# Kernel optimization log

Measured on AMD Instinct MI355X. Metric: run time of the kernel, lower is better.

The kernel has to match this reference:

```python
import jax, jax.numpy as jnp
import numpy as np

D_MODEL = 256
D_STATE = 128          # d_model // 2
D_CONV = 4
EXPAND = 4
D_INNER = EXPAND * D_MODEL  # 1024
DT_RANK = (D_MODEL + 15) // 16  # 16
N_HEADS = 8
D_FF = 4 * D_MODEL
EPS = 1e-6


def layer_norm(x, a, b):
    # torch LayerNorm-like but with unbiased std (ddof=1) per the source
    mean = jnp.mean(x, axis=-1, keepdims=True)
    d = x.shape[-1]
    var = jnp.sum((x - mean) ** 2, axis=-1, keepdims=True) / (d - 1)
    std = jnp.sqrt(var)
    return a * (x - mean) / (std + EPS) + b


def silu(x):
    return x * jax.nn.sigmoid(x)


def mamba(x, in_proj_w, conv_w, conv_b, x_proj_w, dt_proj_w, dt_proj_b, A_log, Dp, out_proj_w):
    B, L, _ = x.shape
    xz = jnp.einsum('bld,ed->ble', x, in_proj_w)  # (B,L,2*D_INNER)
    xi, z = xz[..., :D_INNER], xz[..., D_INNER:]
    # causal depthwise conv1d over L
    xp = jnp.pad(xi, ((0, 0), (D_CONV - 1, 0), (0, 0)))
    u = conv_b
    for k in range(D_CONV):
        u = u + xp[:, k:k + L, :] * conv_w[:, k]
    u = silu(u)  # (B,L,D_INNER)
    dbl = jnp.einsum('bld,ed->ble', u, x_proj_w)  # (B,L,DT_RANK+2*D_STATE)
    dt = dbl[..., :DT_RANK]
    Bm = dbl[..., DT_RANK:DT_RANK + D_STATE]
    Cm = dbl[..., DT_RANK + D_STATE:]
    dt = jax.nn.softplus(jnp.einsum('blr,dr->bld', dt, dt_proj_w) + dt_proj_b)  # (B,L,D_INNER)
    A = -jnp.exp(A_log)  # (D_INNER, D_STATE)
    dA = jnp.exp(jnp.einsum('bld,dn->bldn', dt, A))          # (B,L,Din,N)
    dBu = jnp.einsum('bld,bln,bld->bldn', dt, Bm, u)          # (B,L,Din,N)

    def step(h, inp):
        dA_t, dBu_t, C_t = inp
        h = dA_t * h + dBu_t                    # (B,Din,N)
        y = jnp.einsum('bdn,bn->bd', h, C_t)    # (B,Din)
        return h, y

    h0 = jnp.zeros((B, D_INNER, D_STATE), dtype=x.dtype)
    _, ys = jax.lax.scan(step, h0, (jnp.swapaxes(dA, 0, 1), jnp.swapaxes(dBu, 0, 1), jnp.swapaxes(Cm, 0, 1)))
    y = jnp.swapaxes(ys, 0, 1) + u * Dp  # (B,L,Din)
    y = y * silu(z)
    return jnp.einsum('ble,de->bld', y, out_proj_w)


def cross_attention(q_in, kv_in, mask, wq_w, wq_b, wk_w, wk_b, wv_w, wv_b, wo_w, wo_b):
    B, Lq, _ = q_in.shape
    Lk = kv_in.shape[1]
    dk = D_MODEL // N_HEADS
    q = (jnp.einsum('bld,ed->ble', q_in, wq_w) + wq_b).reshape(B, Lq, N_HEADS, dk).transpose(0, 2, 1, 3)
    k = (jnp.einsum('bld,ed->ble', kv_in, wk_w) + wk_b).reshape(B, Lk, N_HEADS, dk).transpose(0, 2, 1, 3)
    v = (jnp.einsum('bld,ed->ble', kv_in, wv_w) + wv_b).reshape(B, Lk, N_HEADS, dk).transpose(0, 2, 1, 3)
    scores = jnp.einsum('bhqd,bhkd->bhqk', q, k) / np.sqrt(dk)
    # mask: (B,1,Lk) bool -> broadcast (B,1,1,Lk)
    scores = jnp.where(mask[:, None, :, :], scores, jnp.finfo(scores.dtype).min)
    p = jax.nn.softmax(scores, axis=-1)
    o = jnp.einsum('bhqk,bhkd->bhqd', p, v).transpose(0, 2, 1, 3).reshape(B, Lq, D_MODEL)
    return jnp.einsum('ble,de->bld', o, wo_w) + wo_b


def setup_inputs() -> dict:
    key = jax.random.key(0)
    ks = jax.random.split(key, 24)
    s = 0.02
    B, L, Lm = 2, 512, 512
    inp = {
        'x': jax.random.normal(ks[0], (B, L, D_MODEL), jnp.float32),
        'memory': jax.random.normal(ks[1], (B, Lm, D_MODEL), jnp.float32),
        'src_mask': jnp.ones((B, 1, Lm), bool),
        'tgt_mask': jnp.ones((B, 1, L), bool),
        # mamba params
        'in_proj_w': jax.random.normal(ks[2], (2 * D_INNER, D_MODEL)) * s,
        'conv_w': jax.random.normal(ks[3], (D_INNER, D_CONV)) * s,
        'conv_b': jnp.zeros((D_INNER,)),
        'x_proj_w': jax.random.normal(ks[4], (DT_RANK + 2 * D_STATE, D_INNER)) * s,
        'dt_proj_w': jax.random.normal(ks[5], (D_INNER, DT_RANK)) * s,
        'dt_proj_b': jnp.log(jnp.expm1(0.01)) * jnp.ones((D_INNER,)),
        'A_log': jnp.log(jnp.broadcast_to(jnp.arange(1, D_STATE + 1, dtype=jnp.float32), (D_INNER, D_STATE))),
        'Dp': jnp.ones((D_INNER,)),
        'out_proj_w': jax.random.normal(ks[6], (D_MODEL, D_INNER)) * s,
        # norms
        'norm1_a': jnp.ones((D_MODEL,)), 'norm1_b': jnp.zeros((D_MODEL,)),
        'norm2_a': jnp.ones((D_MODEL,)), 'norm2_b': jnp.zeros((D_MODEL,)),
        'norm3_a': jnp.ones((D_MODEL,)), 'norm3_b': jnp.zeros((D_MODEL,)),
        # cross attention
        'wq_w': jax.random.normal(ks[7], (D_MODEL, D_MODEL)) * s, 'wq_b': jnp.zeros((D_MODEL,)),
        'wk_w': jax.random.normal(ks[8], (D_MODEL, D_MODEL)) * s, 'wk_b': jnp.zeros((D_MODEL,)),
        'wv_w': jax.random.normal(ks[9], (D_MODEL, D_MODEL)) * s, 'wv_b': jnp.zeros((D_MODEL,)),
        'wo_w': jax.random.normal(ks[10], (D_MODEL, D_MODEL)) * s, 'wo_b': jnp.zeros((D_MODEL,)),
        # ffn
        'w1_w': jax.random.normal(ks[11], (D_FF, D_MODEL)) * s, 'w1_b': jnp.zeros((D_FF,)),
        'w2_w': jax.random.normal(ks[12], (D_MODEL, D_FF)) * s, 'w2_b': jnp.zeros((D_MODEL,)),
    }
    return inp


def reference(x, memory, src_mask, tgt_mask,
              in_proj_w, conv_w, conv_b, x_proj_w, dt_proj_w, dt_proj_b, A_log, Dp, out_proj_w,
              norm1_a, norm1_b, norm2_a, norm2_b, norm3_a, norm3_b,
              wq_w, wq_b, wk_w, wk_b, wv_w, wv_b, wo_w, wo_b,
              w1_w, w1_b, w2_w, w2_b):
    # self mamba block (pre-norm, residual); dropout = 0
    h = x + mamba(layer_norm(x, norm1_a, norm1_b), in_proj_w, conv_w, conv_b,
                  x_proj_w, dt_proj_w, dt_proj_b, A_log, Dp, out_proj_w)
    # cross attention block
    h = h + cross_attention(layer_norm(h, norm2_a, norm2_b), memory, src_mask,
                            wq_w, wq_b, wk_w, wk_b, wv_w, wv_b, wo_w, wo_b)
    # ffn block
    hn = layer_norm(h, norm3_a, norm3_b)
    ff = jnp.einsum('blf,df->bld', jax.nn.relu(jnp.einsum('bld,fd->blf', hn, w1_w) + w1_b), w2_w) + w2_b
    return h + ff
```

## Files before the change

kernel.cpp:

```cpp
#include <hip/hip_runtime.h>
#include <hip/hip_bf16.h>

#define B_SZ 2
#define L_SEQ 512
#define D_MODEL 256
#define D_STATE 128
#define D_CONV 4
#define D_INNER 1024
#define DT_RANK 16
#define N_HEADS 8
#define DK 32
#define D_FF 1024
#define R_TOT (B_SZ * L_SEQ)
#define DBL_LD (DT_RANK + 2 * D_STATE)
#define NSEG 16
#define SEGL 32
#define DPB 4

typedef __hip_bfloat16 bf16;
typedef __attribute__((ext_vector_type(8))) short short8;
typedef __attribute__((ext_vector_type(4))) float floatx4;

__device__ inline float fexp(float x) { return __expf(x); }
__device__ inline float fexp2(float x) { return __builtin_amdgcn_exp2f(x); }
__device__ inline float frcp(float x) { return __builtin_amdgcn_rcpf(x); }
__device__ inline float silu_f(float x) { return x * frcp(1.f + fexp(-x)); }
__device__ inline float softplus_f(float x) { return (x > 20.f) ? x : __logf(1.f + fexp(x)); }
__device__ inline float bf2f(unsigned short u) { return __uint_as_float(((unsigned)u) << 16); }

__device__ inline float dpp_sum64(float x) {
    x += __int_as_float(__builtin_amdgcn_update_dpp(0, __float_as_int(x), 0x111, 0xf, 0xf, true));
    x += __int_as_float(__builtin_amdgcn_update_dpp(0, __float_as_int(x), 0x112, 0xf, 0xf, true));
    x += __int_as_float(__builtin_amdgcn_update_dpp(0, __float_as_int(x), 0x114, 0xf, 0xf, true));
    x += __int_as_float(__builtin_amdgcn_update_dpp(0, __float_as_int(x), 0x118, 0xf, 0xf, true));
    x += __int_as_float(__builtin_amdgcn_update_dpp(0, __float_as_int(x), 0x142, 0xf, 0xf, true));
    x += __int_as_float(__builtin_amdgcn_update_dpp(0, __float_as_int(x), 0x143, 0xf, 0xf, true));
    return x;
}

__device__ inline float swz_xor16(float x) {
    return __int_as_float(__builtin_amdgcn_ds_swizzle(__float_as_int(x), 0x401F));
}
__device__ inline float swz_xor8(float x) {
    return __int_as_float(__builtin_amdgcn_ds_swizzle(__float_as_int(x), 0x201F));
}

#define S_MEM 262144
#define S_INW 524288
#define S_XPW 278528
#define S_OPW 262144
#define S_WQ  65536
#define S_WK  65536
#define S_WV  65536
#define S_WO  65536
#define S_W1  262144
#define S_W2  262144
#define S_TOT (S_MEM+S_INW+S_XPW+S_OPW+S_WQ+S_WK+S_WV+S_WO+S_W1+S_W2)
#define PACK_BLKS ((S_TOT + 255) / 256)
#define Z1_F4 (4 * R_TOT * D_MODEL / 4)
#define Z2_F4 (R_TOT * D_MODEL / 4)
#define Z3_F4 (R_TOT * DBL_LD / 4)
#define ZERO_BLKS ((Z1_F4 + Z2_F4 + Z3_F4 + 255) / 256)

__global__ __launch_bounds__(256) void pack_ln1(
    const float* __restrict__ s0, const float* __restrict__ s1,
    const float* __restrict__ s2, const float* __restrict__ s3,
    const float* __restrict__ s4, const float* __restrict__ s5,
    const float* __restrict__ s6, const float* __restrict__ s7,
    const float* __restrict__ s8, const float* __restrict__ s9,
    bf16* __restrict__ dst,
    const float* __restrict__ X, const float* __restrict__ a,
    const float* __restrict__ bvec, bf16* __restrict__ ln1b,
    float* __restrict__ zero1, float* __restrict__ zero2,
    float* __restrict__ zero3)
{
    __shared__ float r1[256], r2[256];
    if (blockIdx.x < PACK_BLKS) {
        const long i = (long)blockIdx.x * 256 + threadIdx.x;
        if (i >= S_TOT) return;
        const long off[11] = {0, S_MEM, S_MEM+S_INW, S_MEM+S_INW+S_XPW,
            S_MEM+S_INW+S_XPW+S_OPW, S_MEM+S_INW+S_XPW+S_OPW+S_WQ,
            S_MEM+S_INW+S_XPW+S_OPW+S_WQ+S_WK,
            S_MEM+S_INW+S_XPW+S_OPW+S_WQ+S_WK+S_WV,
            S_MEM+S_INW+S_XPW+S_OPW+S_WQ+S_WK+S_WV+S_WO,
            S_MEM+S_INW+S_XPW+S_OPW+S_WQ+S_WK+S_WV+S_WO+S_W1, S_TOT};
        const float* srcs[10] = {s0,s1,s2,s3,s4,s5,s6,s7,s8,s9};
        int seg = 0;
#pragma unroll
        for (int k = 1; k < 10; ++k) if (i >= off[k]) seg = k;
        dst[i] = __float2bfloat16(srcs[seg][i - off[seg]]);
    } else if (blockIdx.x < PACK_BLKS + R_TOT) {
        const int row = blockIdx.x - PACK_BLKS;
        const int t = threadIdx.x;
        const float v = X[(long)row * D_MODEL + t];
        r1[t] = v;
        r2[t] = v * v;
        __syncthreads();
        for (int s = 128; s > 0; s >>= 1) {
            if (t < s) { r1[t] += r1[t + s]; r2[t] += r2[t + s]; }
            __syncthreads();
        }
        const float mean = r1[0] * (1.f / 256.f);
        const float var = (r2[0] - 256.f * mean * mean) * (1.f / 255.f);
        const float sd = sqrtf(fmaxf(var, 0.f));
        const float o = a[t] * (v - mean) / (sd + 1e-6f) + bvec[t];
        ln1b[(long)row * D_MODEL + t] = __float2bfloat16(o);
    } else {
        const long i4 = (long)(blockIdx.x - PACK_BLKS - R_TOT) * 256 + threadIdx.x;
        const float4 z = {0.f, 0.f, 0.f, 0.f};
        if (i4 < Z1_F4)                      *(float4*)&zero1[i4 * 4] = z;
        else if (i4 < Z1_F4 + Z2_F4)          *(float4*)&zero2[(i4 - Z1_F4) * 4] = z;
        else if (i4 < Z1_F4 + Z2_F4 + Z3_F4)  *(float4*)&zero3[(i4 - Z1_F4 - Z2_F4) * 4] = z;
    }
}

template <int EPI>
__global__ __launch_bounds__(256) void mfma_gemm(
    const bf16* __restrict__ A, const bf16* __restrict__ W, int K,
    float* __restrict__ C, bf16* __restrict__ Cb, int ldc,
    const float* __restrict__ bias, const float* __restrict__ res,
    int M, int N)
{
    const int wave = threadIdx.x >> 6;
    const int lane = threadIdx.x & 63;
    const int row16 = lane & 15;
    const int quad  = lane >> 4;
    const int bm = blockIdx.y * 64 + wave * 16;
    const int bn = blockIdx.x * 64;

    floatx4 acc[4];
#pragma unroll
    for (int t = 0; t < 4; ++t) acc[t] = (floatx4){0.f, 0.f, 0.f, 0.f};

    const long arow = (long)(bm + row16) * K;
    for (int k0 = 0; k0 < K; k0 += 32) {
        const short8 av = *(const short8*)(A + arow + k0 + quad * 8);
#pragma unroll
        for (int t = 0; t < 4; ++t) {
            const int gn = bn + t * 16 + row16;
            short8 bv = {0,0,0,0,0,0,0,0};
            if (gn < N) bv = *(const short8*)(W + (long)gn * K + k0 + quad * 8);
            acc[t] = __builtin_amdgcn_mfma_f32_16x16x32_bf16(av, bv, acc[t], 0, 0, 0);
        }
    }

#pragma unroll
    for (int t = 0; t < 4; ++t) {
        const int gn = bn + t * 16 + row16;
        if (gn >= N) continue;
        const float bs = bias ? bias[gn] : 0.f;
#pragma unroll
        for (int r = 0; r < 4; ++r) {
            const int gm = bm + quad * 4 + r;
            float v = acc[t][r] + bs;
            if (EPI == 1) v = fmaxf(v, 0.f);
            const long ci = (long)gm * ldc + gn;
            if (res) v += res[ci];
            if (C)  C[ci] = v;
            if (Cb) Cb[ci] = __float2bfloat16(v);
        }
    }
}

template <int SK>
__global__ __launch_bounds__(256) void splitk_gemm(
    const bf16* __restrict__ A, const bf16* __restrict__ W, int K,
    float* __restrict__ C, int ldc,
    const float* __restrict__ bias, const float* __restrict__ res,
    int M, int N)
{
    const int wave = threadIdx.x >> 6;
    const int lane = threadIdx.x & 63;
    const int row16 = lane & 15;
    const int quad  = lane >> 4;
    const int bm = blockIdx.y * 64 + wave * 16;
    const int bn = blockIdx.x * 64;
    const int kz = blockIdx.z;
    const int ksl = K / SK;
    const int kbeg = kz * ksl;

    floatx4 acc[4];
#pragma unroll
    for (int t = 0; t < 4; ++t) acc[t] = (floatx4){0.f, 0.f, 0.f, 0.f};

    const long arow = (long)(bm + row16) * K;
    for (int k0 = kbeg; k0 < kbeg + ksl; k0 += 32) {
        const short8 av = *(const short8*)(A + arow + k0 + quad * 8);
#pragma unroll
        for (int t = 0; t < 4; ++t) {
            const int gn = bn + t * 16 + row16;
            short8 bv = {0,0,0,0,0,0,0,0};
            if (gn < N) bv = *(const short8*)(W + (long)gn * K + k0 + quad * 8);
            acc[t] = __builtin_amdgcn_mfma_f32_16x16x32_bf16(av, bv, acc[t], 0, 0, 0);
        }
    }

#pragma unroll
    for (int t = 0; t < 4; ++t) {
        const int gn = bn + t * 16 + row16;
        if (gn >= N) continue;
        const float bs = (kz == 0 && bias) ? bias[gn] : 0.f;
#pragma unroll
        for (int r = 0; r < 4; ++r) {
            const int gm = bm + quad * 4 + r;
            float v = acc[t][r] + bs;
            const long ci = (long)gm * ldc + gn;
            if (kz == 0 && res) v += res[ci];
            atomicAdd(&C[ci], v);
        }
    }
}

__global__ __launch_bounds__(256) void xproj_kv_gemm(
    const bf16* __restrict__ ub, const bf16* __restrict__ XPWb,
    float* __restrict__ dbl,
    const bf16* __restrict__ memb, const bf16* __restrict__ WKb,
    const bf16* __restrict__ WVb,
    const float* __restrict__ WKB, const float* __restrict__ WVB,
    float* __restrict__ kb, float* __restrict__ vb)
{
    const int wave = threadIdx.x >> 6;
    const int lane = threadIdx.x & 63;
    const int row16 = lane & 15;
    const int quad  = lane >> 4;
    const int bm = blockIdx.y * 64 + wave * 16;
    const int bn = blockIdx.x * 64;
    const int z = blockIdx.z;

    const bf16* A; const bf16* W; const float* bias; float* C;
    int K, N, ldc, kbeg, ksl;
    if (z < 4) {
        A = ub; W = XPWb; bias = nullptr; C = dbl;
        K = D_INNER; N = DBL_LD; ldc = DBL_LD;
        ksl = D_INNER / 4; kbeg = z * ksl;
    } else {
        if (bn >= D_MODEL) return;
        const int zz = z - 4;
        const int which = zz >> 1;
        const int kz = zz & 1;
        A = memb; W = which ? WVb : WKb;
        bias = (kz == 0) ? (which ? WVB : WKB) : nullptr;
        C = which ? vb : kb;
        K = D_MODEL; N = D_MODEL; ldc = D_MODEL;
        ksl = D_MODEL / 2; kbeg = kz * ksl;
    }

    floatx4 acc[4];
#pragma unroll
    for (int t = 0; t < 4; ++t) acc[t] = (floatx4){0.f, 0.f, 0.f, 0.f};

    const long arow = (long)(bm + row16) * K;
    for (int k0 = kbeg; k0 < kbeg + ksl; k0 += 32) {
        const short8 av = *(const short8*)(A + arow + k0 + quad * 8);
#pragma unroll
        for (int t = 0; t < 4; ++t) {
            const int gn = bn + t * 16 + row16;
            short8 bv = {0,0,0,0,0,0,0,0};
            if (gn < N) bv = *(const short8*)(W + (long)gn * K + k0 + quad * 8);
            acc[t] = __builtin_amdgcn_mfma_f32_16x16x32_bf16(av, bv, acc[t], 0, 0, 0);
        }
    }

#pragma unroll
    for (int t = 0; t < 4; ++t) {
        const int gn = bn + t * 16 + row16;
        if (gn >= N) continue;
        const float bs = bias ? bias[gn] : 0.f;
#pragma unroll
        for (int r = 0; r < 4; ++r) {
            const int gm = bm + quad * 4 + r;
            atomicAdd(&C[(long)gm * ldc + gn], acc[t][r] + bs);
        }
    }
}

__global__ __launch_bounds__(256) void q_gemm(
    const bf16* __restrict__ ln2b, const bf16* __restrict__ WQb,
    const float* __restrict__ WQB, float* __restrict__ qb)
{
    const int wave = threadIdx.x >> 6;
    const int lane = threadIdx.x & 63;
    const int row16 = lane & 15;
    const int quad  = lane >> 4;
    const int bm = blockIdx.y * 64 + wave * 16;
    const int bn = blockIdx.x * 64;
    const int kz = blockIdx.z;
    const int kbeg = kz * (D_MODEL / 2);

    floatx4 acc[4];
#pragma unroll
    for (int t = 0; t < 4; ++t) acc[t] = (floatx4){0.f, 0.f, 0.f, 0.f};

    const long arow = (long)(bm + row16) * D_MODEL;
    for (int k0 = kbeg; k0 < kbeg + D_MODEL / 2; k0 += 32) {
        const short8 av = *(const short8*)(ln2b + arow + k0 + quad * 8);
#pragma unroll
        for (int t = 0; t < 4; ++t) {
            const int gn = bn + t * 16 + row16;
            const short8 bv = *(const short8*)(WQb + (long)gn * D_MODEL + k0 + quad * 8);
            acc[t] = __builtin_amdgcn_mfma_f32_16x16x32_bf16(av, bv, acc[t], 0, 0, 0);
        }
    }
#pragma unroll
    for (int t = 0; t < 4; ++t) {
        const int gn = bn + t * 16 + row16;
        const float bs = (kz == 0) ? WQB[gn] : 0.f;
#pragma unroll
        for (int r = 0; r < 4; ++r) {
            const int gm = bm + quad * 4 + r;
            atomicAdd(&qb[(long)gm * D_MODEL + gn], acc[t][r] + bs);
        }
    }
}

__global__ __launch_bounds__(256) void gemm16_ln(
    const bf16* __restrict__ A, const bf16* __restrict__ W, int K,
    const float* __restrict__ bias, const float* __restrict__ res,
    float* __restrict__ Cf,
    const float* __restrict__ lna, const float* __restrict__ lnb,
    bf16* __restrict__ lnout)
{
    __shared__ float tile[16][264];
    __shared__ float red1[16][16];
    __shared__ float red2[16][16];
    const int w = threadIdx.x >> 6;
    const int lane = threadIdx.x & 63;
    const int row16 = lane & 15;
    const int quad  = lane >> 4;
    const int bm = blockIdx.x * 16;

    floatx4 acc[4];
#pragma unroll
    for (int t = 0; t < 4; ++t) acc[t] = (floatx4){0.f, 0.f, 0.f, 0.f};

    const long arow = (long)(bm + row16) * K;
    for (int k0 = 0; k0 < K; k0 += 32) {
        const short8 av = *(const short8*)(A + arow + k0 + quad * 8);
#pragma unroll
        for (int t = 0; t < 4; ++t) {
            const int gn = w * 64 + t * 16 + row16;
            const short8 bv = *(const short8*)(W + (long)gn * K + k0 + quad * 8);
            acc[t] = __builtin_amdgcn_mfma_f32_16x16x32_bf16(av, bv, acc[t], 0, 0, 0);
        }
    }

#pragma unroll
    for (int t = 0; t < 4; ++t) {
        const int gn = w * 64 + t * 16 + row16;
        const float bs = bias ? bias[gn] : 0.f;
#pragma unroll
        for (int r = 0; r < 4; ++r) {
            const int gm = bm + quad * 4 + r;
            float v = acc[t][r] + bs;
            const long ci = (long)gm * D_MODEL + gn;
            if (res) v += res[ci];
            Cf[ci] = v;
            tile[quad * 4 + r][gn] = v;
        }
    }
    __syncthreads();

    const int r = threadIdx.x >> 4;
    const int g = threadIdx.x & 15;
    float s = 0.f, q = 0.f;
#pragma unroll
    for (int i = 0; i < 16; ++i) {
        const float x = tile[r][g * 16 + i];
        s += x; q += x * x;
    }
    red1[r][g] = s; red2[r][g] = q;
    __syncthreads();
    float ts = 0.f, tq = 0.f;
#pragma unroll
    for (int i = 0; i < 16; ++i) { ts += red1[r][i]; tq += red2[r][i]; }
    const float mean = ts * (1.f / 256.f);
    const float var = (tq - 256.f * mean * mean) * (1.f / 255.f);
    const float sd = sqrtf(fmaxf(var, 0.f));
    const long rowbase = (long)(bm + r) * D_MODEL;
#pragma unroll
    for (int i = 0; i < 16; ++i) {
        const int c = g * 16 + i;
        const float o = lna[c] * (tile[r][c] - mean) / (sd + 1e-6f) + lnb[c];
        lnout[rowbase + c] = __float2bfloat16(o);
    }
}

__global__ __launch_bounds__(256) void ln_kernel(
    const float* __restrict__ x, const float* __restrict__ a,
    const float* __restrict__ bvec, bf16* __restrict__ out)
{
    const int row = blockIdx.x;
    const int t = threadIdx.x;
    const float v = x[(long)row * D_MODEL + t];
    __shared__ float r1[256], r2[256];
    r1[t] = v;
    r2[t] = v * v;
    __syncthreads();
    for (int s = 128; s > 0; s >>= 1) {
        if (t < s) { r1[t] += r1[t + s]; r2[t] += r2[t + s]; }
        __syncthreads();
    }
    const float mean = r1[0] * (1.f / 256.f);
    const float var = (r2[0] - 256.f * mean * mean) * (1.f / 255.f);
    const float sd = sqrtf(fmaxf(var, 0.f));
    const float o = a[t] * (v - mean) / (sd + 1e-6f) + bvec[t];
    out[(long)row * D_MODEL + t] = __float2bfloat16(o);
}

__global__ __launch_bounds__(256) void dt_gemm_T(
    const float* __restrict__ A , const float* __restrict__ W ,
    const float* __restrict__ bias, float* __restrict__ dtT)
{
    __shared__ float As[DT_RANK][65];
    __shared__ float Bs[DT_RANK][65];
    __shared__ float Ct[64][65];
    const int bm = blockIdx.y * 64;
    const int bn = blockIdx.x * 64;
    const int tid = threadIdx.x;
    const int tx = tid & 15;
    const int ty = tid >> 4;
    const int r = tid >> 2;
    const int kk = (tid & 3) * 4;
#pragma unroll
    for (int q = 0; q < 4; ++q) {
        As[kk + q][r] = A[(long)(bm + r) * DBL_LD + kk + q];
        Bs[kk + q][r] = W[(long)(bn + r) * DT_RANK + kk + q];
    }
    __syncthreads();
    float acc[4][4] = {};
#pragma unroll
    for (int k = 0; k < DT_RANK; ++k) {
        float a[4], bv[4];
#pragma unroll
        for (int i = 0; i < 4; ++i) a[i] = As[k][ty * 4 + i];
#pragma unroll
        for (int j = 0; j < 4; ++j) bv[j] = Bs[k][tx * 4 + j];
#pragma unroll
        for (int i = 0; i < 4; ++i)
#pragma unroll
            for (int j = 0; j < 4; ++j)
                acc[i][j] = fmaf(a[i], bv[j], acc[i][j]);
    }
#pragma unroll
    for (int i = 0; i < 4; ++i)
#pragma unroll
        for (int j = 0; j < 4; ++j)
            Ct[tx * 4 + j][ty * 4 + i] = softplus_f(acc[i][j] + bias[bn + tx * 4 + j]);
    __syncthreads();
    const int b = bm >> 9;
    const int l0 = bm & 511;
    const int r2 = tid >> 4;
    const int c4 = (tid & 15) * 4;
#pragma unroll
    for (int q = 0; q < 4; ++q) {
        const int dl = r2 + q * 16;
        float4 v = {Ct[dl][c4], Ct[dl][c4 + 1], Ct[dl][c4 + 2], Ct[dl][c4 + 3]};
        *(float4*)&dtT[((long)(b * D_INNER + bn + dl) << 9) + l0 + c4] = v;
    }
}

__global__ __launch_bounds__(256) void conv_silu_T(
    const bf16* __restrict__ xz, const float* __restrict__ cw,
    const float* __restrict__ cb, bf16* __restrict__ ub, float* __restrict__ uT)
{
    __shared__ float t[64][65];
    const int db = blockIdx.x;
    const int lb = blockIdx.y;
    const int b  = blockIdx.z;
    const int tid = threadIdx.x;
    const int r  = tid >> 4;
    const int c4 = (tid & 15) * 4;
    const int d0 = db * 64 + c4;

    const float4 cb4 = *(const float4*)&cb[d0];
    float cwa[4][4];
#pragma unroll
    for (int i = 0; i < 4; ++i) {
        const float4 w = *(const float4*)&cw[(d0 + i) * 4];
        cwa[i][0] = w.x; cwa[i][1] = w.y; cwa[i][2] = w.z; cwa[i][3] = w.w;
    }

#pragma unroll
    for (int q = 0; q < 4; ++q) {
        const int ll = r + q * 16;
        const int l = lb * 64 + ll;
        float s0 = cb4.x, s1 = cb4.y, s2 = cb4.z, s3 = cb4.w;
#pragma unroll
        for (int k = 0; k < D_CONV; ++k) {
            const int ls = l - 3 + k;
            if (ls >= 0) {
                const ushort4 xv = *(const ushort4*)&xz[((long)(b * L_SEQ + ls)) * (2 * D_INNER) + d0];
                s0 = fmaf(bf2f(xv.x), cwa[0][k], s0);
                s1 = fmaf(bf2f(xv.y), cwa[1][k], s1);
                s2 = fmaf(bf2f(xv.z), cwa[2][k], s2);
                s3 = fmaf(bf2f(xv.w), cwa[3][k], s3);
            }
        }
        s0 = silu_f(s0); s1 = silu_f(s1); s2 = silu_f(s2); s3 = silu_f(s3);
        bf16 b0 = __float2bfloat16(s0), b1 = __float2bfloat16(s1);
        bf16 b2 = __float2bfloat16(s2), b3 = __float2bfloat16(s3);
        ushort4 pk;
        pk.x = *reinterpret_cast<unsigned short*>(&b0);
        pk.y = *reinterpret_cast<unsigned short*>(&b1);
        pk.z = *reinterpret_cast<unsigned short*>(&b2);
        pk.w = *reinterpret_cast<unsigned short*>(&b3);
        *reinterpret_cast<ushort4*>(ub + ((long)(b * L_SEQ + l)) * D_INNER + d0) = pk;
        t[c4 + 0][ll] = s0; t[c4 + 1][ll] = s1;
        t[c4 + 2][ll] = s2; t[c4 + 3][ll] = s3;
    }
    __syncthreads();
#pragma unroll
    for (int q = 0; q < 4; ++q) {
        const int dl = r + q * 16;
        float4 v = {t[dl][c4], t[dl][c4 + 1], t[dl][c4 + 2], t[dl][c4 + 3]};
        *(float4*)&uT[((long)(b * D_INNER + db * 64 + dl) << 9) + lb * 64 + c4] = v;
    }
}

__global__ __launch_bounds__(1024) void scan_fused(
    const float* __restrict__ dtT, const float* __restrict__ uT,
    const float* __restrict__ dbl, const float* __restrict__ A_log,
    float* __restrict__ ysT)
{
    const int b  = blockIdx.x >> 8;
    const int d0 = (blockIdx.x & 255) * DPB;
    const int w = threadIdx.x >> 6;
    const int lane = threadIdx.x & 63;
    const int n0 = lane * 2;

    __shared__ float Sh[NSEG][DPB][D_STATE];
    __shared__ float Ph[NSEG][DPB][D_STATE];

    float An0[DPB], An1[DPB];
#pragma unroll
    for (int di = 0; di < DPB; ++di) {
        An0[di] = -fexp(A_log[(long)(d0 + di) * D_STATE + n0]) * 1.44269504f;
        An1[di] = -fexp(A_log[(long)(d0 + di) * D_STATE + n0 + 1]) * 1.44269504f;
    }

    const float* blp = dbl + ((long)(b * L_SEQ + w * SEGL)) * DBL_LD + DT_RANK + n0;
    const float* clp = blp + D_STATE;
    const long tbase = ((long)(b * D_INNER + d0) << 9) + w * SEGL;

    if (w < NSEG - 1) {
        float h0[DPB] = {}, h1[DPB] = {}, sdt[DPB] = {};
        for (int s = 0; s < SEGL / 8; ++s) {
            float2 Bv[8];
#pragma unroll
            for (int j = 0; j < 8; ++j)
                Bv[j] = *(const float2*)(blp + (long)(s * 8 + j) * DBL_LD);
#pragma unroll
            for (int di = 0; di < DPB; ++di) {
                const float* dtp = dtT + tbase + ((long)di << 9) + s * 8;
                const float* up  = uT  + tbase + ((long)di << 9) + s * 8;
                const float4 dt0 = *(const float4*)dtp;
                const float4 dt1 = *(const float4*)(dtp + 4);
                const float4 u0  = *(const float4*)up;
                const float4 u1  = *(const float4*)(up + 4);
                const float dts[8] = {dt0.x, dt0.y, dt0.z, dt0.w, dt1.x, dt1.y, dt1.z, dt1.w};
                const float us[8]  = {u0.x,  u0.y,  u0.z,  u0.w,  u1.x,  u1.y,  u1.z,  u1.w};
#pragma unroll
                for (int j = 0; j < 8; ++j) {
                    const float dtv = dts[j];
                    sdt[di] += dtv;
                    const float dtu = dtv * us[j];
                    h0[di] = fmaf(fexp2(dtv * An0[di]), h0[di], dtu * Bv[j].x);
                    h1[di] = fmaf(fexp2(dtv * An1[di]), h1[di], dtu * Bv[j].y);
                }
            }
        }
#pragma unroll
        for (int di = 0; di < DPB; ++di) {
            Sh[w][di][n0]     = h0[di];
            Sh[w][di][n0 + 1] = h1[di];
            Ph[w][di][n0]     = fexp2(An0[di] * sdt[di]);
            Ph[w][di][n0 + 1] = fexp2(An1[di] * sdt[di]);
        }
    }
    __syncthreads();

    float h0[DPB] = {}, h1[DPB] = {};
    for (int s = 0; s < w; ++s) {
#pragma unroll
        for (int di = 0; di < DPB; ++di) {
            h0[di] = fmaf(Ph[s][di][n0],     h0[di], Sh[s][di][n0]);
            h1[di] = fmaf(Ph[s][di][n0 + 1], h1[di], Sh[s][di][n0 + 1]);
        }
    }

    const int bpa = (lane ^ 32) << 2;
    const bool lo32 = lane < 32;
    const bool b16 = (lane & 16) != 0;
    const bool b8  = (lane & 8) != 0;
    const int g = lane >> 3;
    const bool wl = (lane & 7) == 7;

    for (int s = 0; s < SEGL / 8; ++s) {
        float2 Bv[8], Cv[8];
#pragma unroll
        for (int j = 0; j < 8; ++j) {
            Bv[j] = *(const float2*)(blp + (long)(s * 8 + j) * DBL_LD);
            Cv[j] = *(const float2*)(clp + (long)(s * 8 + j) * DBL_LD);
        }
#pragma unroll
        for (int di = 0; di < DPB; ++di) {
            const float* dtp = dtT + tbase + ((long)di << 9) + s * 8;
            const float* up  = uT  + tbase + ((long)di << 9) + s * 8;
            const float4 dt0 = *(const float4*)dtp;
            const float4 dt1 = *(const float4*)(dtp + 4);
            const float4 u0  = *(const float4*)up;
            const float4 u1  = *(const float4*)(up + 4);
            const float dts[8] = {dt0.x, dt0.y, dt0.z, dt0.w, dt1.x, dt1.y, dt1.z, dt1.w};
            const float us[8]  = {u0.x,  u0.y,  u0.z,  u0.w,  u1.x,  u1.y,  u1.z,  u1.w};
            float yp[8];
#pragma unroll
            for (int j = 0; j < 8; ++j) {
                const float dtv = dts[j];
                const float dtu = dtv * us[j];
                h0[di] = fmaf(fexp2(dtv * An0[di]), h0[di], dtu * Bv[j].x);
                h1[di] = fmaf(fexp2(dtv * An1[di]), h1[di], dtu * Bv[j].y);
                yp[j] = fmaf(h0[di], Cv[j].x, h1[di] * Cv[j].y);
            }
            float z0[4];
#pragma unroll
            for (int j = 0; j < 4; ++j) {
                const float t = lo32 ? yp[j]     : yp[j + 4];
                const float u = lo32 ? yp[j + 4] : yp[j];
                z0[j] = t + __int_as_float(
                    __builtin_amdgcn_ds_bpermute(bpa, __float_as_int(u)));
            }
            float z1[2];
#pragma unroll
            for (int j = 0; j < 2; ++j) {
                const float t = b16 ? z0[j + 2] : z0[j];
                const float u = b16 ? z0[j]     : z0[j + 2];
                z1[j] = t + swz_xor16(u);
            }
            float z2;
            {
                const float t = b8 ? z1[1] : z1[0];
                const float u = b8 ? z1[0] : z1[1];
                z2 = t + swz_xor8(u);
            }
            z2 += __int_as_float(__builtin_amdgcn_update_dpp(0, __float_as_int(z2), 0x111, 0xf, 0xf, true));
            z2 += __int_as_float(__builtin_amdgcn_update_dpp(0, __float_as_int(z2), 0x112, 0xf, 0xf, true));
            z2 += __int_as_float(__builtin_amdgcn_update_dpp(0, __float_as_int(z2), 0x114, 0xf, 0xf, true));
            if (wl) ysT[tbase + ((long)di << 9) + s * 8 + g] = z2;
        }
    }
}

__global__ __launch_bounds__(256) void gate_kernel(
    const float* __restrict__ ysT, const float* __restrict__ uT,
    const float* __restrict__ Dp, const bf16* __restrict__ xz,
    bf16* __restrict__ y)
{
    __shared__ float t[64][65];
    __shared__ float t2[64][65];
    const int db = blockIdx.x;
    const int lb = blockIdx.y;
    const int b  = blockIdx.z;
    const int tid = threadIdx.x;
    const int r  = tid >> 4;
    const int c4 = (tid & 15) * 4;

#pragma unroll
    for (int q = 0; q < 4; ++q) {
        const int dr = r + q * 16;
        const long base = (((long)(b * D_INNER + db * 64 + dr)) << 9) + lb * 64 + c4;
        const float4 v = *(const float4*)&ysT[base];
        const float4 w = *(const float4*)&uT[base];
        t[dr][c4 + 0] = v.x; t[dr][c4 + 1] = v.y;
        t[dr][c4 + 2] = v.z; t[dr][c4 + 3] = v.w;
        t2[dr][c4 + 0] = w.x; t2[dr][c4 + 1] = w.y;
        t2[dr][c4 + 2] = w.z; t2[dr][c4 + 3] = w.w;
    }
    __syncthreads();

    const float4 dp4 = *(const float4*)&Dp[db * 64 + c4];
#pragma unroll
    for (int q = 0; q < 4; ++q) {
        const int lr = r + q * 16;
        const long row = (long)b * L_SEQ + lb * 64 + lr;
        const ushort4 zu = *(const ushort4*)&xz[row * 2 * D_INNER + D_INNER + db * 64 + c4];
        const float r0 = (t[c4 + 0][lr] + t2[c4 + 0][lr] * dp4.x) * silu_f(bf2f(zu.x));
        const float r1 = (t[c4 + 1][lr] + t2[c4 + 1][lr] * dp4.y) * silu_f(bf2f(zu.y));
        const float r2 = (t[c4 + 2][lr] + t2[c4 + 2][lr] * dp4.z) * silu_f(bf2f(zu.z));
        const float r3 = (t[c4 + 3][lr] + t2[c4 + 3][lr] * dp4.w) * silu_f(bf2f(zu.w));
        bf16 b0 = __float2bfloat16(r0), b1 = __float2bfloat16(r1);
        bf16 b2 = __float2bfloat16(r2), b3 = __float2bfloat16(r3);
        ushort4 pk;
        pk.x = *reinterpret_cast<unsigned short*>(&b0);
        pk.y = *reinterpret_cast<unsigned short*>(&b1);
        pk.z = *reinterpret_cast<unsigned short*>(&b2);
        pk.w = *reinterpret_cast<unsigned short*>(&b3);
        *reinterpret_cast<ushort4*>(y + row * D_INNER + db * 64 + c4) = pk;
    }
}

#define QT 16
#define CK 64

__global__ __launch_bounds__(256) void attn_kernel(
    const float* __restrict__ q, const float* __restrict__ k,
    const float* __restrict__ v, bf16* __restrict__ o)
{
    const int qt = blockIdx.x;
    const int hh = blockIdx.y;
    const int b  = blockIdx.z;
    const int t = threadIdx.x;
    const int lane = t & 15;
    const int qa = t >> 4;
    const int q0 = qt * QT + qa;

    __shared__ float Ks[CK][36];
    __shared__ float Vs[CK][36];

    const float scale = 0.17677669529663687f;
    float qr0[32];
    {
        const float* q0p = q + ((long)(b * L_SEQ + q0) * D_MODEL + hh * DK);
#pragma unroll
        for (int i = 0; i < 8; ++i) {
            const float4 a = *(const float4*)&q0p[i * 4];
            qr0[i*4+0] = a.x * scale; qr0[i*4+1] = a.y * scale;
            qr0[i*4+2] = a.z * scale; qr0[i*4+3] = a.w * scale;
        }
    }

    float m0 = -1e30f, l0 = 0.f, o0[32] = {};

    for (int c = 0; c < L_SEQ; c += CK) {
        __syncthreads();
        {
            const int fid = t * 2;
            const int row = fid >> 3;
            const int c0  = (fid & 7) * 4;
            const float* kp = k + ((long)(b * L_SEQ + c + row) * D_MODEL + hh * DK + c0);
            const float* vp = v + ((long)(b * L_SEQ + c + row) * D_MODEL + hh * DK + c0);
            *(float4*)&Ks[row][c0]     = *(const float4*)kp;
            *(float4*)&Ks[row][c0 + 4] = *(const float4*)(kp + 4);
            *(float4*)&Vs[row][c0]     = *(const float4*)vp;
            *(float4*)&Vs[row][c0 + 4] = *(const float4*)(vp + 4);
        }
        __syncthreads();

        float s0[4];
#pragma unroll
        for (int i = 0; i < 4; ++i) {
            const int kk = i * 16 + lane;
            float a0 = 0.f;
#pragma unroll
            for (int dd = 0; dd < 32; dd += 4) {
                const float4 kv = *(const float4*)&Ks[kk][dd];
                a0 = fmaf(qr0[dd+0], kv.x, a0); a0 = fmaf(qr0[dd+1], kv.y, a0);
                a0 = fmaf(qr0[dd+2], kv.z, a0); a0 = fmaf(qr0[dd+3], kv.w, a0);
            }
            s0[i] = a0;
        }

        float cm0 = s0[0];
#pragma unroll
        for (int i = 1; i < 4; ++i) cm0 = fmaxf(cm0, s0[i]);
#pragma unroll
        for (int off = 8; off > 0; off >>= 1)
            cm0 = fmaxf(cm0, __shfl_down(cm0, off, 16));
        cm0 = __shfl(cm0, 0, 16);

        const float nm0 = fmaxf(m0, cm0);
        const float al0 = fexp(m0 - nm0);
        l0 *= al0;
#pragma unroll
        for (int dd = 0; dd < 32; ++dd) o0[dd] *= al0;
        m0 = nm0;

        float p0[4];
#pragma unroll
        for (int i = 0; i < 4; ++i) { p0[i] = fexp(s0[i] - m0); l0 += p0[i]; }

#pragma unroll
        for (int i = 0; i < 4; ++i) {
            const int kk = i * 16 + lane;
#pragma unroll
            for (int dd = 0; dd < 32; dd += 4) {
                const float4 vv = *(const float4*)&Vs[kk][dd];
                o0[dd+0] = fmaf(p0[i], vv.x, o0[dd+0]);
                o0[dd+1] = fmaf(p0[i], vv.y, o0[dd+1]);
                o0[dd+2] = fmaf(p0[i], vv.z, o0[dd+2]);
                o0[dd+3] = fmaf(p0[i], vv.w, o0[dd+3]);
            }
        }
    }

#pragma unroll
    for (int off = 8; off > 0; off >>= 1) {
        l0 += __shfl_down(l0, off, 16);
#pragma unroll
        for (int dd = 0; dd < 32; ++dd) o0[dd] += __shfl_down(o0[dd], off, 16);
    }
    if (lane == 0) {
        const float i0 = 1.f / l0;
        bf16* op0 = o + ((long)(b * L_SEQ + q0) * D_MODEL + hh * DK);
#pragma unroll
        for (int dd = 0; dd < 32; ++dd) op0[dd] = __float2bfloat16(o0[dd] * i0);
    }
}


extern "C" void kernel_launch(void* const* d_in, const int* in_sizes, int n_in,
                              void* d_out, int out_size, void* d_ws, size_t ws_size,
                              hipStream_t stream) {
    const float* X   = (const float*)d_in[0];
    const float* MEM = (const float*)d_in[1];
    const float* CW  = (const float*)d_in[5];
    const float* CB  = (const float*)d_in[6];
    const float* DTW = (const float*)d_in[8];
    const float* DTB = (const float*)d_in[9];
    const float* ALG = (const float*)d_in[10];
    const float* DP  = (const float*)d_in[11];
    const float* N1A = (const float*)d_in[13];
    const float* N1B = (const float*)d_in[14];
    const float* N2A = (const float*)d_in[15];
    const float* N2B = (const float*)d_in[16];
    const float* N3A = (const float*)d_in[17];
    const float* N3B = (const float*)d_in[18];
    const float* WQB = (const float*)d_in[20];
    const float* WKB = (const float*)d_in[22];
    const float* WVB = (const float*)d_in[24];
    const float* WOB = (const float*)d_in[26];
    const float* W1B = (const float*)d_in[28];
    const float* W2B = (const float*)d_in[30];
    const float* INW = (const float*)d_in[4];
    const float* XPW = (const float*)d_in[7];
    const float* OPW = (const float*)d_in[12];
    const float* WQ  = (const float*)d_in[19];
    const float* WKw = (const float*)d_in[21];
    const float* WVw = (const float*)d_in[23];
    const float* WO  = (const float*)d_in[25];
    const float* W1  = (const float*)d_in[27];
    const float* W2  = (const float*)d_in[29];
    float* out = (float*)d_out;

    bf16* bp = (bf16*)d_ws;
    bf16* ub   = bp;  bp += (long)R_TOT * D_INNER;
    bf16* ybb  = bp;  bp += (long)R_TOT * D_INNER;
    bf16* ffab = ybb;
    bf16* xzb  = bp;  bp += (long)R_TOT * 2 * D_INNER;
    bf16* ln1b = bp;  bp += (long)R_TOT * D_MODEL;
    bf16* aob  = ln1b;
    bf16* ln2b = bp;  bp += (long)R_TOT * D_MODEL;
    bf16* ln3b = ln2b;
    bf16* arena = bp; bp += S_TOT;
    bf16* MEMb = arena;
    bf16* INWb = MEMb + S_MEM;
    bf16* XPWb = INWb + S_INW;
    bf16* OPWb = XPWb + S_XPW;
    bf16* WQb  = OPWb + S_OPW;
    bf16* WKb  = WQb + S_WQ;
    bf16* WVb  = WKb + S_WK;
    bf16* WOb  = WVb + S_WV;
    bf16* W1b  = WOb + S_WO;
    bf16* W2b  = W1b + S_W1;

    float* p = (float*)(bp + ((((long)(bp - (bf16*)d_ws)) & 1) ? 1 : 0));
    float* uT  = p;                                  p += (long)R_TOT * D_INNER;
    float* dbl = p;                                  p += (long)R_TOT * DBL_LD;
    float* dtT = p;                                  p += (long)R_TOT * D_INNER;
    float* ysT = p;                                  p += (long)R_TOT * D_INNER;
    float* h1  = p;                                  p += (long)R_TOT * D_MODEL;
    float* qb  = p;                                  p += (long)R_TOT * D_MODEL;
    float* kb  = p;                                  p += (long)R_TOT * D_MODEL;
    float* vb  = p;                                  p += (long)R_TOT * D_MODEL;
    float* h2  = p;                                  p += (long)R_TOT * D_MODEL;

    const dim3 blk256(256);
    const int MT64 = R_TOT / 64;

    pack_ln1<<<PACK_BLKS + R_TOT + ZERO_BLKS, blk256, 0, stream>>>(
        MEM, INW, XPW, OPW, WQ, WKw, WVw, WO, W1, W2, arena,
        X, N1A, N1B, ln1b, h1, out, dbl);

    mfma_gemm<0><<<dim3(2 * D_INNER / 64, MT64), blk256, 0, stream>>>(
        ln1b, INWb, D_MODEL, nullptr, xzb, 2 * D_INNER, nullptr, nullptr,
        R_TOT, 2 * D_INNER);

    conv_silu_T<<<dim3(D_INNER / 64, L_SEQ / 64, B_SZ), blk256, 0, stream>>>(
        xzb, CW, CB, ub, uT);

    xproj_kv_gemm<<<dim3((DBL_LD + 63) / 64, MT64, 8), blk256, 0, stream>>>(
        ub, XPWb, dbl, MEMb, WKb, WVb, WKB, WVB, kb, vb);

    dt_gemm_T<<<dim3(D_INNER / 64, MT64), blk256, 0, stream>>>(dbl, DTW, DTB, dtT);

    scan_fused<<<B_SZ * D_INNER / DPB, dim3(1024), 0, stream>>>(dtT, uT, dbl, ALG, ysT);

    gate_kernel<<<dim3(D_INNER / 64, L_SEQ / 64, B_SZ), blk256, 0, stream>>>(
        ysT, uT, DP, xzb, ybb);

    splitk_gemm<4><<<dim3(D_MODEL / 64, MT64, 4), blk256, 0, stream>>>(
        ybb, OPWb, D_INNER, h1, D_MODEL, nullptr, X, R_TOT, D_MODEL);

    ln_kernel<<<R_TOT, blk256, 0, stream>>>(h1, N2A, N2B, ln2b);

    q_gemm<<<dim3(D_MODEL / 64, MT64, 2), blk256, 0, stream>>>(ln2b, WQb, WQB, qb);

    attn_kernel<<<dim3(L_SEQ / QT, N_HEADS, B_SZ), blk256, 0, stream>>>(qb, kb, vb, aob);

    gemm16_ln<<<R_TOT / 16, blk256, 0, stream>>>(
        aob, WOb, D_MODEL, WOB, h1, h2, N3A, N3B, ln3b);

    mfma_gemm<1><<<dim3(D_FF / 64, MT64), blk256, 0, stream>>>(
        ln3b, W1b, D_MODEL, nullptr, ffab, D_FF, W1B, nullptr, R_TOT, D_FF);

    splitk_gemm<4><<<dim3(D_MODEL / 64, MT64, 4), blk256, 0, stream>>>(
        ffab, W2b, D_FF, out, D_MODEL, W2B, h2, R_TOT, D_MODEL);

    (void)in_sizes; (void)n_in; (void)out_size; (void)ws_size;
}
```

Baseline: 321.8 us.

## Merge pre-scan and post-scan kernel chains into two cooperative persistent kernels

Replaces the chain of separate launches before the scan (pack/LN1, in_proj GEMM, conv+SiLU, x_proj/KV GEMM, dt GEMM) and after it (gate, out_proj, LN2, Q, attention, WO+LN3, FFN) with two cooperative kernels. Inside each, grid-stride loops run the former stages and grid.sync() separates them. The goal is to cut kernel launch overhead and inter-kernel gaps across the many small stages. In exchange, the grid is capped by occupancy, each stage runs at one fixed grid size and shared-memory footprint, and grid-wide barriers add their own cost.

```diff
diff --git a/kernel.cpp b/kernel.cpp
--- a/kernel.cpp
+++ b/kernel.cpp
@@ -1,5 +1,8 @@
 #include <hip/hip_runtime.h>
 #include <hip/hip_bf16.h>
+#include <hip/hip_cooperative_groups.h>
+
+namespace cg = cooperative_groups;
 
 #define B_SZ 2
 #define L_SEQ 512
@@ -28,21 +31,29 @@
 __device__ inline float softplus_f(float x) { return (x > 20.f) ? x : __logf(1.f + fexp(x)); }
 __device__ inline float bf2f(unsigned short u) { return __uint_as_float(((unsigned)u) << 16); }
 
-__device__ inline float dpp_sum64(float x) {
-    x += __int_as_float(__builtin_amdgcn_update_dpp(0, __float_as_int(x), 0x111, 0xf, 0xf, true));
-    x += __int_as_float(__builtin_amdgcn_update_dpp(0, __float_as_int(x), 0x112, 0xf, 0xf, true));
-    x += __int_as_float(__builtin_amdgcn_update_dpp(0, __float_as_int(x), 0x114, 0xf, 0xf, true));
-    x += __int_as_float(__builtin_amdgcn_update_dpp(0, __float_as_int(x), 0x118, 0xf, 0xf, true));
-    x += __int_as_float(__builtin_amdgcn_update_dpp(0, __float_as_int(x), 0x142, 0xf, 0xf, true));
-    x += __int_as_float(__builtin_amdgcn_update_dpp(0, __float_as_int(x), 0x143, 0xf, 0xf, true));
-    return x;
-}
-
 __device__ inline float swz_xor16(float x) {
     return __int_as_float(__builtin_amdgcn_ds_swizzle(__float_as_int(x), 0x401F));
 }
 __device__ inline float swz_xor8(float x) {
     return __int_as_float(__builtin_amdgcn_ds_swizzle(__float_as_int(x), 0x201F));
+}
+
+__device__ inline void gemm64_body(const bf16* A, const bf16* W, int K,
+    int kbeg, int kend, int bm, int bn, int N, floatx4 acc[4], int lane)
+{
+    const int row16 = lane & 15;
+    const int quad  = lane >> 4;
+    const long arow = (long)(bm + row16) * K;
+    for (int k0 = kbeg; k0 < kend; k0 += 32) {
+        const short8 av = *(const short8*)(A + arow + k0 + quad * 8);
+#pragma unroll
+        for (int t = 0; t < 4; ++t) {
+            const int gn = bn + t * 16 + row16;
+            short8 bv = {0,0,0,0,0,0,0,0};
+            if (gn < N) bv = *(const short8*)(W + (long)gn * K + k0 + quad * 8);
+            acc[t] = __builtin_amdgcn_mfma_f32_16x16x32_bf16(av, bv, acc[t], 0, 0, 0);
+        }
+    }
 }
 
 #define S_MEM 262144
@@ -62,458 +73,237 @@
 #define Z3_F4 (R_TOT * DBL_LD / 4)
 #define ZERO_BLKS ((Z1_F4 + Z2_F4 + Z3_F4 + 255) / 256)
 
-__global__ __launch_bounds__(256) void pack_ln1(
-    const float* __restrict__ s0, const float* __restrict__ s1,
-    const float* __restrict__ s2, const float* __restrict__ s3,
-    const float* __restrict__ s4, const float* __restrict__ s5,
-    const float* __restrict__ s6, const float* __restrict__ s7,
-    const float* __restrict__ s8, const float* __restrict__ s9,
-    bf16* __restrict__ dst,
-    const float* __restrict__ X, const float* __restrict__ a,
-    const float* __restrict__ bvec, bf16* __restrict__ ln1b,
-    float* __restrict__ zero1, float* __restrict__ zero2,
-    float* __restrict__ zero3)
+__global__ __launch_bounds__(256, 4) void head_fused(
+    const float* s0, const float* s1, const float* s2, const float* s3,
+    const float* s4, const float* s5, const float* s6, const float* s7,
+    const float* s8, const float* s9,
+    bf16* arena,
+    const float* X, const float* n1a, const float* n1b, bf16* ln1b,
+    float* z1, float* z2, float* z3,
+    const bf16* INWb, bf16* xzb,
+    const float* CW, const float* CB, bf16* ub, float* uT,
+    const bf16* XPWb, float* dbl,
+    const bf16* MEMb, const bf16* WKb, const bf16* WVb,
+    const float* WKB, const float* WVB, float* kb, float* vbuf,
+    const float* DTW, const float* DTB, float* dtT)
 {
-    __shared__ float r1[256], r2[256];
-    if (blockIdx.x < PACK_BLKS) {
-        const long i = (long)blockIdx.x * 256 + threadIdx.x;
-        if (i >= S_TOT) return;
-        const long off[11] = {0, S_MEM, S_MEM+S_INW, S_MEM+S_INW+S_XPW,
-            S_MEM+S_INW+S_XPW+S_OPW, S_MEM+S_INW+S_XPW+S_OPW+S_WQ,
-            S_MEM+S_INW+S_XPW+S_OPW+S_WQ+S_WK,
-            S_MEM+S_INW+S_XPW+S_OPW+S_WQ+S_WK+S_WV,
-            S_MEM+S_INW+S_XPW+S_OPW+S_WQ+S_WK+S_WV+S_WO,
-            S_MEM+S_INW+S_XPW+S_OPW+S_WQ+S_WK+S_WV+S_WO+S_W1, S_TOT};
-        const float* srcs[10] = {s0,s1,s2,s3,s4,s5,s6,s7,s8,s9};
-        int seg = 0;
-#pragma unroll
-        for (int k = 1; k < 10; ++k) if (i >= off[k]) seg = k;
-        dst[i] = __float2bfloat16(srcs[seg][i - off[seg]]);
-    } else if (blockIdx.x < PACK_BLKS + R_TOT) {
-        const int row = blockIdx.x - PACK_BLKS;
-        const int t = threadIdx.x;
-        const float v = X[(long)row * D_MODEL + t];
-        r1[t] = v;
-        r2[t] = v * v;
-        __syncthreads();
-        for (int s = 128; s > 0; s >>= 1) {
-            if (t < s) { r1[t] += r1[t + s]; r2[t] += r2[t + s]; }
-            __syncthreads();
-        }
-        const float mean = r1[0] * (1.f / 256.f);
-        const float var = (r2[0] - 256.f * mean * mean) * (1.f / 255.f);
-        const float sd = sqrtf(fmaxf(var, 0.f));
-        const float o = a[t] * (v - mean) / (sd + 1e-6f) + bvec[t];
-        ln1b[(long)row * D_MODEL + t] = __float2bfloat16(o);
-    } else {
-        const long i4 = (long)(blockIdx.x - PACK_BLKS - R_TOT) * 256 + threadIdx.x;
-        const float4 z = {0.f, 0.f, 0.f, 0.f};
-        if (i4 < Z1_F4)                      *(float4*)&zero1[i4 * 4] = z;
-        else if (i4 < Z1_F4 + Z2_F4)          *(float4*)&zero2[(i4 - Z1_F4) * 4] = z;
-        else if (i4 < Z1_F4 + Z2_F4 + Z3_F4)  *(float4*)&zero3[(i4 - Z1_F4 - Z2_F4) * 4] = z;
-    }
-}
-
-template <int EPI>
-__global__ __launch_bounds__(256) void mfma_gemm(
-    const bf16* __restrict__ A, const bf16* __restrict__ W, int K,
-    float* __restrict__ C, bf16* __restrict__ Cb, int ldc,
-    const float* __restrict__ bias, const float* __restrict__ res,
-    int M, int N)
-{
-    const int wave = threadIdx.x >> 6;
-    const int lane = threadIdx.x & 63;
+    cg::grid_group gg = cg::this_grid();
+    __shared__ float sm[6240];
+    const int tid = threadIdx.x;
+    const int NB = (int)gridDim.x;
+    const int lane = tid & 63;
+    const int wave = tid >> 6;
     const int row16 = lane & 15;
     const int quad  = lane >> 4;
-    const int bm = blockIdx.y * 64 + wave * 16;
-    const int bn = blockIdx.x * 64;
-
-    floatx4 acc[4];
-#pragma unroll
-    for (int t = 0; t < 4; ++t) acc[t] = (floatx4){0.f, 0.f, 0.f, 0.f};
-
-    const long arow = (long)(bm + row16) * K;
-    for (int k0 = 0; k0 < K; k0 += 32) {
-        const short8 av = *(const short8*)(A + arow + k0 + quad * 8);
+
+    {
+        const int TOTB = PACK_BLKS + R_TOT + ZERO_BLKS;
+        for (int vb0 = (int)blockIdx.x; vb0 < TOTB; vb0 += NB) {
+            if (vb0 < PACK_BLKS) {
+                const long i = (long)vb0 * 256 + tid;
+                if (i < S_TOT) {
+                    const long off[11] = {0, S_MEM, S_MEM+S_INW, S_MEM+S_INW+S_XPW,
+                        S_MEM+S_INW+S_XPW+S_OPW, S_MEM+S_INW+S_XPW+S_OPW+S_WQ,
+                        S_MEM+S_INW+S_XPW+S_OPW+S_WQ+S_WK,
+                        S_MEM+S_INW+S_XPW+S_OPW+S_WQ+S_WK+S_WV,
+                        S_MEM+S_INW+S_XPW+S_OPW+S_WQ+S_WK+S_WV+S_WO,
+                        S_MEM+S_INW+S_XPW+S_OPW+S_WQ+S_WK+S_WV+S_WO+S_W1, S_TOT};
+                    const float* srcs[10] = {s0,s1,s2,s3,s4,s5,s6,s7,s8,s9};
+                    int seg = 0;
+#pragma unroll
+                    for (int k = 1; k < 10; ++k) if (i >= off[k]) seg = k;
+                    arena[i] = __float2bfloat16(srcs[seg][i - off[seg]]);
+                }
+            } else if (vb0 < PACK_BLKS + R_TOT) {
+                float* r1 = sm; float* r2 = sm + 256;
+                const int row = vb0 - PACK_BLKS;
+                const float v = X[(long)row * D_MODEL + tid];
+                r1[tid] = v; r2[tid] = v * v;
+                __syncthreads();
+                for (int s = 128; s > 0; s >>= 1) {
+                    if (tid < s) { r1[tid] += r1[tid + s]; r2[tid] += r2[tid + s]; }
+                    __syncthreads();
+                }
+                const float mean = r1[0] * (1.f / 256.f);
+                const float var = (r2[0] - 256.f * mean * mean) * (1.f / 255.f);
+                const float sd = sqrtf(fmaxf(var, 0.f));
+                const float o = n1a[tid] * (v - mean) / (sd + 1e-6f) + n1b[tid];
+                ln1b[(long)row * D_MODEL + tid] = __float2bfloat16(o);
+                __syncthreads();
+            } else {
+                const long i4 = (long)(vb0 - PACK_BLKS - R_TOT) * 256 + tid;
+                const float4 zz = {0.f, 0.f, 0.f, 0.f};
+                if (i4 < Z1_F4)                      *(float4*)&z1[i4 * 4] = zz;
+                else if (i4 < Z1_F4 + Z2_F4)          *(float4*)&z2[(i4 - Z1_F4) * 4] = zz;
+                else if (i4 < Z1_F4 + Z2_F4 + Z3_F4)  *(float4*)&z3[(i4 - Z1_F4 - Z2_F4) * 4] = zz;
+            }
+        }
+    }
+    gg.sync();
+
+    for (int vb0 = (int)blockIdx.x; vb0 < 512; vb0 += NB) {
+        const int bn = (vb0 & 31) * 64;
+        const int bm = (vb0 >> 5) * 64 + wave * 16;
+        floatx4 acc[4];
+#pragma unroll
+        for (int t = 0; t < 4; ++t) acc[t] = (floatx4){0.f, 0.f, 0.f, 0.f};
+        gemm64_body(ln1b, INWb, D_MODEL, 0, D_MODEL, bm, bn, 2 * D_INNER, acc, lane);
 #pragma unroll
         for (int t = 0; t < 4; ++t) {
             const int gn = bn + t * 16 + row16;
-            short8 bv = {0,0,0,0,0,0,0,0};
-            if (gn < N) bv = *(const short8*)(W + (long)gn * K + k0 + quad * 8);
-            acc[t] = __builtin_amdgcn_mfma_f32_16x16x32_bf16(av, bv, acc[t], 0, 0, 0);
-        }
-    }
-
-#pragma unroll
-    for (int t = 0; t < 4; ++t) {
-        const int gn = bn + t * 16 + row16;
-        if (gn >= N) continue;
-        const float bs = bias ? bias[gn] : 0.f;
-#pragma unroll
-        for (int r = 0; r < 4; ++r) {
-            const int gm = bm + quad * 4 + r;
-            float v = acc[t][r] + bs;
-            if (EPI == 1) v = fmaxf(v, 0.f);
-            const long ci = (long)gm * ldc + gn;
-            if (res) v += res[ci];
-            if (C)  C[ci] = v;
-            if (Cb) Cb[ci] = __float2bfloat16(v);
-        }
-    }
-}
-
-template <int SK>
-__global__ __launch_bounds__(256) void splitk_gemm(
-    const bf16* __restrict__ A, const bf16* __restrict__ W, int K,
-    float* __restrict__ C, int ldc,
-    const float* __restrict__ bias, const float* __restrict__ res,
-    int M, int N)
-{
-    const int wave = threadIdx.x >> 6;
-    const int lane = threadIdx.x & 63;
-    const int row16 = lane & 15;
-    const int quad  = lane >> 4;
-    const int bm = blockIdx.y * 64 + wave * 16;
-    const int bn = blockIdx.x * 64;
-    const int kz = blockIdx.z;
-    const int ksl = K / SK;
-    const int kbeg = kz * ksl;
-
-    floatx4 acc[4];
-#pragma unroll
-    for (int t = 0; t < 4; ++t) acc[t] = (floatx4){0.f, 0.f, 0.f, 0.f};
-
-    const long arow = (long)(bm + row16) * K;
-    for (int k0 = kbeg; k0 < kbeg + ksl; k0 += 32) {
-        const short8 av = *(const short8*)(A + arow + k0 + quad * 8);
+#pragma unroll
+            for (int r = 0; r < 4; ++r) {
+                const int gm = bm + quad * 4 + r;
+                xzb[(long)gm * (2 * D_INNER) + gn] = __float2bfloat16(acc[t][r]);
+            }
+        }
+    }
+    gg.sync();
+
+    for (int vb0 = (int)blockIdx.x; vb0 < 256; vb0 += NB) {
+        float (*tt)[65] = (float(*)[65])sm;
+        const int db = vb0 & 15;
+        const int lb = (vb0 >> 4) & 7;
+        const int b  = vb0 >> 7;
+        const int r  = tid >> 4;
+        const int c4 = (tid & 15) * 4;
+        const int d0 = db * 64 + c4;
+
+        const float4 cb4 = *(const float4*)&CB[d0];
+        float cwa[4][4];
+#pragma unroll
+        for (int i = 0; i < 4; ++i) {
+            const float4 w4 = *(const float4*)&CW[(d0 + i) * 4];
+            cwa[i][0] = w4.x; cwa[i][1] = w4.y; cwa[i][2] = w4.z; cwa[i][3] = w4.w;
+        }
+#pragma unroll
+        for (int q = 0; q < 4; ++q) {
+            const int ll = r + q * 16;
+            const int l = lb * 64 + ll;
+            float v0 = cb4.x, v1 = cb4.y, v2 = cb4.z, v3 = cb4.w;
+#pragma unroll
+            for (int k = 0; k < D_CONV; ++k) {
+                const int ls = l - 3 + k;
+                if (ls >= 0) {
+                    const ushort4 xv = *(const ushort4*)&xzb[((long)(b * L_SEQ + ls)) * (2 * D_INNER) + d0];
+                    v0 = fmaf(bf2f(xv.x), cwa[0][k], v0);
+                    v1 = fmaf(bf2f(xv.y), cwa[1][k], v1);
+                    v2 = fmaf(bf2f(xv.z), cwa[2][k], v2);
+                    v3 = fmaf(bf2f(xv.w), cwa[3][k], v3);
+                }
+            }
+            v0 = silu_f(v0); v1 = silu_f(v1); v2 = silu_f(v2); v3 = silu_f(v3);
+            bf16 b0 = __float2bfloat16(v0), b1 = __float2bfloat16(v1);
+            bf16 b2 = __float2bfloat16(v2), b3 = __float2bfloat16(v3);
+            ushort4 pk;
+            pk.x = *reinterpret_cast<unsigned short*>(&b0);
+            pk.y = *reinterpret_cast<unsigned short*>(&b1);
+            pk.z = *reinterpret_cast<unsigned short*>(&b2);
+            pk.w = *reinterpret_cast<unsigned short*>(&b3);
+            *reinterpret_cast<ushort4*>(ub + ((long)(b * L_SEQ + l)) * D_INNER + d0) = pk;
+            tt[c4 + 0][ll] = v0; tt[c4 + 1][ll] = v1;
+            tt[c4 + 2][ll] = v2; tt[c4 + 3][ll] = v3;
+        }
+        __syncthreads();
+#pragma unroll
+        for (int q = 0; q < 4; ++q) {
+            const int dl = r + q * 16;
+            float4 v = {tt[dl][c4], tt[dl][c4 + 1], tt[dl][c4 + 2], tt[dl][c4 + 3]};
+            *(float4*)&uT[((long)(b * D_INNER + db * 64 + dl) << 9) + lb * 64 + c4] = v;
+        }
+        __syncthreads();
+    }
+    gg.sync();
+
+    for (int vb0 = (int)blockIdx.x; vb0 < 640; vb0 += NB) {
+        const int xib = vb0 % 5;
+        const int yib = (vb0 / 5) & 15;
+        const int z   = vb0 / 80;
+        const int bm = yib * 64 + wave * 16;
+        const int bn = xib * 64;
+
+        const bf16* A; const bf16* W; const float* bias; float* C;
+        int K, N, ldc, kbeg, ksl;
+        if (z < 4) {
+            A = ub; W = XPWb; bias = nullptr; C = dbl;
+            K = D_INNER; N = DBL_LD; ldc = DBL_LD;
+            ksl = D_INNER / 4; kbeg = z * ksl;
+        } else {
+            if (bn >= D_MODEL) continue;
+            const int zz = z - 4;
+            const int which = zz >> 1;
+            const int kz = zz & 1;
+            A = MEMb; W = which ? WVb : WKb;
+            bias = (kz == 0) ? (which ? WVB : WKB) : nullptr;
+            C = which ? vbuf : kb;
+            K = D_MODEL; N = D_MODEL; ldc = D_MODEL;
+            ksl = D_MODEL / 2; kbeg = kz * ksl;
+        }
+        floatx4 acc[4];
+#pragma unroll
+        for (int t = 0; t < 4; ++t) acc[t] = (floatx4){0.f, 0.f, 0.f, 0.f};
+        gemm64_body(A, W, K, kbeg, kbeg + ksl, bm, bn, N, acc, lane);
 #pragma unroll
         for (int t = 0; t < 4; ++t) {
             const int gn = bn + t * 16 + row16;
-            short8 bv = {0,0,0,0,0,0,0,0};
-            if (gn < N) bv = *(const short8*)(W + (long)gn * K + k0 + quad * 8);
-            acc[t] = __builtin_amdgcn_mfma_f32_16x16x32_bf16(av, bv, acc[t], 0, 0, 0);
-        }
-    }
-
-#pragma unroll
-    for (int t = 0; t < 4; ++t) {
-        const int gn = bn + t * 16 + row16;
-        if (gn >= N) continue;
-        const float bs = (kz == 0 && bias) ? bias[gn] : 0.f;
-#pragma unroll
-        for (int r = 0; r < 4; ++r) {
-            const int gm = bm + quad * 4 + r;
-            float v = acc[t][r] + bs;
-            const long ci = (long)gm * ldc + gn;
-            if (kz == 0 && res) v += res[ci];
-            atomicAdd(&C[ci], v);
-        }
-    }
-}
-
-__global__ __launch_bounds__(256) void xproj_kv_gemm(
-    const bf16* __restrict__ ub, const bf16* __restrict__ XPWb,
-    float* __restrict__ dbl,
-    const bf16* __restrict__ memb, const bf16* __restrict__ WKb,
-    const bf16* __restrict__ WVb,
-    const float* __restrict__ WKB, const float* __restrict__ WVB,
-    float* __restrict__ kb, float* __restrict__ vb)
-{
-    const int wave = threadIdx.x >> 6;
-    const int lane = threadIdx.x & 63;
-    const int row16 = lane & 15;
-    const int quad  = lane >> 4;
-    const int bm = blockIdx.y * 64 + wave * 16;
-    const int bn = blockIdx.x * 64;
-    const int z = blockIdx.z;
-
-    const bf16* A; const bf16* W; const float* bias; float* C;
-    int K, N, ldc, kbeg, ksl;
-    if (z < 4) {
-        A = ub; W = XPWb; bias = nullptr; C = dbl;
-        K = D_INNER; N = DBL_LD; ldc = DBL_LD;
-        ksl = D_INNER / 4; kbeg = z * ksl;
-    } else {
-        if (bn >= D_MODEL) return;
-        const int zz = z - 4;
-        const int which = zz >> 1;
-        const int kz = zz & 1;
-        A = memb; W = which ? WVb : WKb;
-        bias = (kz == 0) ? (which ? WVB : WKB) : nullptr;
-        C = which ? vb : kb;
-        K = D_MODEL; N = D_MODEL; ldc = D_MODEL;
-        ksl = D_MODEL / 2; kbeg = kz * ksl;
-    }
-
-    floatx4 acc[4];
-#pragma unroll
-    for (int t = 0; t < 4; ++t) acc[t] = (floatx4){0.f, 0.f, 0.f, 0.f};
-
-    const long arow = (long)(bm + row16) * K;
-    for (int k0 = kbeg; k0 < kbeg + ksl; k0 += 32) {
-        const short8 av = *(const short8*)(A + arow + k0 + quad * 8);
-#pragma unroll
-        for (int t = 0; t < 4; ++t) {
-            const int gn = bn + t * 16 + row16;
-            short8 bv = {0,0,0,0,0,0,0,0};
-            if (gn < N) bv = *(const short8*)(W + (long)gn * K + k0 + quad * 8);
-            acc[t] = __builtin_amdgcn_mfma_f32_16x16x32_bf16(av, bv, acc[t], 0, 0, 0);
-        }
-    }
-
-#pragma unroll
-    for (int t = 0; t < 4; ++t) {
-        const int gn = bn + t * 16 + row16;
-        if (gn >= N) continue;
-        const float bs = bias ? bias[gn] : 0.f;
-#pragma unroll
-        for (int r = 0; r < 4; ++r) {
-            const int gm = bm + quad * 4 + r;
-            atomicAdd(&C[(long)gm * ldc + gn], acc[t][r] + bs);
-        }
-    }
-}
-
-__global__ __launch_bounds__(256) void q_gemm(
-    const bf16* __restrict__ ln2b, const bf16* __restrict__ WQb,
-    const float* __restrict__ WQB, float* __restrict__ qb)
-{
-    const int wave = threadIdx.x >> 6;
-    const int lane = threadIdx.x & 63;
-    const int row16 = lane & 15;
-    const int quad  = lane >> 4;
-    const int bm = blockIdx.y * 64 + wave * 16;
-    const int bn = blockIdx.x * 64;
-    const int kz = blockIdx.z;
-    const int kbeg = kz * (D_MODEL / 2);
-
-    floatx4 acc[4];
-#pragma unroll
-    for (int t = 0; t < 4; ++t) acc[t] = (floatx4){0.f, 0.f, 0.f, 0.f};
-
-    const long arow = (long)(bm + row16) * D_MODEL;
-    for (int k0 = kbeg; k0 < kbeg + D_MODEL / 2; k0 += 32) {
-        const short8 av = *(const short8*)(ln2b + arow + k0 + quad * 8);
-#pragma unroll
-        for (int t = 0; t < 4; ++t) {
-            const int gn = bn + t * 16 + row16;
-            const short8 bv = *(const short8*)(WQb + (long)gn * D_MODEL + k0 + quad * 8);
-            acc[t] = __builtin_amdgcn_mfma_f32_16x16x32_bf16(av, bv, acc[t], 0, 0, 0);
-        }
-    }
-#pragma unroll
-    for (int t = 0; t < 4; ++t) {
-        const int gn = bn + t * 16 + row16;
-        const float bs = (kz == 0) ? WQB[gn] : 0.f;
-#pragma unroll
-        for (int r = 0; r < 4; ++r) {
-            const int gm = bm + quad * 4 + r;
-            atomicAdd(&qb[(long)gm * D_MODEL + gn], acc[t][r] + bs);
-        }
-    }
-}
-
-__global__ __launch_bounds__(256) void gemm16_ln(
-    const bf16* __restrict__ A, const bf16* __restrict__ W, int K,
-    const float* __restrict__ bias, const float* __restrict__ res,
-    float* __restrict__ Cf,
-    const float* __restrict__ lna, const float* __restrict__ lnb,
-    bf16* __restrict__ lnout)
-{
-    __shared__ float tile[16][264];
-    __shared__ float red1[16][16];
-    __shared__ float red2[16][16];
-    const int w = threadIdx.x >> 6;
-    const int lane = threadIdx.x & 63;
-    const int row16 = lane & 15;
-    const int quad  = lane >> 4;
-    const int bm = blockIdx.x * 16;
-
-    floatx4 acc[4];
-#pragma unroll
-    for (int t = 0; t < 4; ++t) acc[t] = (floatx4){0.f, 0.f, 0.f, 0.f};
-
-    const long arow = (long)(bm + row16) * K;
-    for (int k0 = 0; k0 < K; k0 += 32) {
-        const short8 av = *(const short8*)(A + arow + k0 + quad * 8);
-#pragma unroll
-        for (int t = 0; t < 4; ++t) {
-            const int gn = w * 64 + t * 16 + row16;
-            const short8 bv = *(const short8*)(W + (long)gn * K + k0 + quad * 8);
-            acc[t] = __builtin_amdgcn_mfma_f32_16x16x32_bf16(av, bv, acc[t], 0, 0, 0);
-        }
-    }
-
-#pragma unroll
-    for (int t = 0; t < 4; ++t) {
-        const int gn = w * 64 + t * 16 + row16;
-        const float bs = bias ? bias[gn] : 0.f;
-#pragma unroll
-        for (int r = 0; r < 4; ++r) {
-            const int gm = bm + quad * 4 + r;
-            float v = acc[t][r] + bs;
-            const long ci = (long)gm * D_MODEL + gn;
-            if (res) v += res[ci];
-            Cf[ci] = v;
-            tile[quad * 4 + r][gn] = v;
-        }
-    }
-    __syncthreads();
-
-    const int r = threadIdx.x >> 4;
-    const int g = threadIdx.x & 15;
-    float s = 0.f, q = 0.f;
-#pragma unroll
-    for (int i = 0; i < 16; ++i) {
-        const float x = tile[r][g * 16 + i];
-        s += x; q += x * x;
-    }
-    red1[r][g] = s; red2[r][g] = q;
-    __syncthreads();
-    float ts = 0.f, tq = 0.f;
-#pragma unroll
-    for (int i = 0; i < 16; ++i) { ts += red1[r][i]; tq += red2[r][i]; }
-    const float mean = ts * (1.f / 256.f);
-    const float var = (tq - 256.f * mean * mean) * (1.f / 255.f);
-    const float sd = sqrtf(fmaxf(var, 0.f));
-    const long rowbase = (long)(bm + r) * D_MODEL;
-#pragma unroll
-    for (int i = 0; i < 16; ++i) {
-        const int c = g * 16 + i;
-        const float o = lna[c] * (tile[r][c] - mean) / (sd + 1e-6f) + lnb[c];
-        lnout[rowbase + c] = __float2bfloat16(o);
-    }
-}
-
-__global__ __launch_bounds__(256) void ln_kernel(
-    const float* __restrict__ x, const float* __restrict__ a,
-    const float* __restrict__ bvec, bf16* __restrict__ out)
-{
-    const int row = blockIdx.x;
-    const int t = threadIdx.x;
-    const float v = x[(long)row * D_MODEL + t];
-    __shared__ float r1[256], r2[256];
-    r1[t] = v;
-    r2[t] = v * v;
-    __syncthreads();
-    for (int s = 128; s > 0; s >>= 1) {
-        if (t < s) { r1[t] += r1[t + s]; r2[t] += r2[t + s]; }
-        __syncthreads();
-    }
-    const float mean = r1[0] * (1.f / 256.f);
-    const float var = (r2[0] - 256.f * mean * mean) * (1.f / 255.f);
-    const float sd = sqrtf(fmaxf(var, 0.f));
-    const float o = a[t] * (v - mean) / (sd + 1e-6f) + bvec[t];
-    out[(long)row * D_MODEL + t] = __float2bfloat16(o);
-}
-
-__global__ __launch_bounds__(256) void dt_gemm_T(
-    const float* __restrict__ A , const float* __restrict__ W ,
-    const float* __restrict__ bias, float* __restrict__ dtT)
-{
-    __shared__ float As[DT_RANK][65];
-    __shared__ float Bs[DT_RANK][65];
-    __shared__ float Ct[64][65];
-    const int bm = blockIdx.y * 64;
-    const int bn = blockIdx.x * 64;
-    const int tid = threadIdx.x;
-    const int tx = tid & 15;
-    const int ty = tid >> 4;
-    const int r = tid >> 2;
-    const int kk = (tid & 3) * 4;
-#pragma unroll
-    for (int q = 0; q < 4; ++q) {
-        As[kk + q][r] = A[(long)(bm + r) * DBL_LD + kk + q];
-        Bs[kk + q][r] = W[(long)(bn + r) * DT_RANK + kk + q];
-    }
-    __syncthreads();
-    float acc[4][4] = {};
-#pragma unroll
-    for (int k = 0; k < DT_RANK; ++k) {
-        float a[4], bv[4];
-#pragma unroll
-        for (int i = 0; i < 4; ++i) a[i] = As[k][ty * 4 + i];
-#pragma unroll
-        for (int j = 0; j < 4; ++j) bv[j] = Bs[k][tx * 4 + j];
+            if (gn >= N) continue;
+            const float bs = bias ? bias[gn] : 0.f;
+#pragma unroll
+            for (int r = 0; r < 4; ++r) {
+                const int gm = bm + quad * 4 + r;
+                atomicAdd(&C[(long)gm * ldc + gn], acc[t][r] + bs);
+            }
+        }
+    }
+    gg.sync();
+
+    for (int vb0 = (int)blockIdx.x; vb0 < 256; vb0 += NB) {
+        float (*As)[65] = (float(*)[65])sm;
+        float (*Bs)[65] = (float(*)[65])(sm + 1040);
+        float (*Ct)[65] = (float(*)[65])(sm + 2080);
+        const int bm = (vb0 >> 4) * 64;
+        const int bn = (vb0 & 15) * 64;
+        const int tx = tid & 15;
+        const int ty = tid >> 4;
+        const int r = tid >> 2;
+        const int kk = (tid & 3) * 4;
+#pragma unroll
+        for (int q = 0; q < 4; ++q) {
+            As[kk + q][r] = dbl[(long)(bm + r) * DBL_LD + kk + q];
+            Bs[kk + q][r] = DTW[(long)(bn + r) * DT_RANK + kk + q];
+        }
+        __syncthreads();
+        float acc[4][4] = {};
+#pragma unroll
+        for (int k = 0; k < DT_RANK; ++k) {
+            float a[4], bv[4];
+#pragma unroll
+            for (int i = 0; i < 4; ++i) a[i] = As[k][ty * 4 + i];
+#pragma unroll
+            for (int j = 0; j < 4; ++j) bv[j] = Bs[k][tx * 4 + j];
+#pragma unroll
+            for (int i = 0; i < 4; ++i)
+#pragma unroll
+                for (int j = 0; j < 4; ++j)
+                    acc[i][j] = fmaf(a[i], bv[j], acc[i][j]);
+        }
 #pragma unroll
         for (int i = 0; i < 4; ++i)
 #pragma unroll
             for (int j = 0; j < 4; ++j)
-                acc[i][j] = fmaf(a[i], bv[j], acc[i][j]);
-    }
-#pragma unroll
-    for (int i = 0; i < 4; ++i)
-#pragma unroll
-        for (int j = 0; j < 4; ++j)
-            Ct[tx * 4 + j][ty * 4 + i] = softplus_f(acc[i][j] + bias[bn + tx * 4 + j]);
-    __syncthreads();
-    const int b = bm >> 9;
-    const int l0 = bm & 511;
-    const int r2 = tid >> 4;
-    const int c4 = (tid & 15) * 4;
-#pragma unroll
-    for (int q = 0; q < 4; ++q) {
-        const int dl = r2 + q * 16;
-        float4 v = {Ct[dl][c4], Ct[dl][c4 + 1], Ct[dl][c4 + 2], Ct[dl][c4 + 3]};
-        *(float4*)&dtT[((long)(b * D_INNER + bn + dl) << 9) + l0 + c4] = v;
-    }
-}
-
-__global__ __launch_bounds__(256) void conv_silu_T(
-    const bf16* __restrict__ xz, const float* __restrict__ cw,
-    const float* __restrict__ cb, bf16* __restrict__ ub, float* __restrict__ uT)
-{
-    __shared__ float t[64][65];
-    const int db = blockIdx.x;
-    const int lb = blockIdx.y;
-    const int b  = blockIdx.z;
-    const int tid = threadIdx.x;
-    const int r  = tid >> 4;
-    const int c4 = (tid & 15) * 4;
-    const int d0 = db * 64 + c4;
-
-    const float4 cb4 = *(const float4*)&cb[d0];
-    float cwa[4][4];
-#pragma unroll
-    for (int i = 0; i < 4; ++i) {
-        const float4 w = *(const float4*)&cw[(d0 + i) * 4];
-        cwa[i][0] = w.x; cwa[i][1] = w.y; cwa[i][2] = w.z; cwa[i][3] = w.w;
-    }
-
-#pragma unroll
-    for (int q = 0; q < 4; ++q) {
-        const int ll = r + q * 16;
-        const int l = lb * 64 + ll;
-        float s0 = cb4.x, s1 = cb4.y, s2 = cb4.z, s3 = cb4.w;
-#pragma unroll
-        for (int k = 0; k < D_CONV; ++k) {
-            const int ls = l - 3 + k;
-            if (ls >= 0) {
-                const ushort4 xv = *(const ushort4*)&xz[((long)(b * L_SEQ + ls)) * (2 * D_INNER) + d0];
-                s0 = fmaf(bf2f(xv.x), cwa[0][k], s0);
-                s1 = fmaf(bf2f(xv.y), cwa[1][k], s1);
-                s2 = fmaf(bf2f(xv.z), cwa[2][k], s2);
-                s3 = fmaf(bf2f(xv.w), cwa[3][k], s3);
-            }
-        }
-        s0 = silu_f(s0); s1 = silu_f(s1); s2 = silu_f(s2); s3 = silu_f(s3);
-        bf16 b0 = __float2bfloat16(s0), b1 = __float2bfloat16(s1);
-        bf16 b2 = __float2bfloat16(s2), b3 = __float2bfloat16(s3);
-        ushort4 pk;
-        pk.x = *reinterpret_cast<unsigned short*>(&b0);
-        pk.y = *reinterpret_cast<unsigned short*>(&b1);
-        pk.z = *reinterpret_cast<unsigned short*>(&b2);
-        pk.w = *reinterpret_cast<unsigned short*>(&b3);
-        *reinterpret_cast<ushort4*>(ub + ((long)(b * L_SEQ + l)) * D_INNER + d0) = pk;
-        t[c4 + 0][ll] = s0; t[c4 + 1][ll] = s1;
-        t[c4 + 2][ll] = s2; t[c4 + 3][ll] = s3;
-    }
-    __syncthreads();
-#pragma unroll
-    for (int q = 0; q < 4; ++q) {
-        const int dl = r + q * 16;
-        float4 v = {t[dl][c4], t[dl][c4 + 1], t[dl][c4 + 2], t[dl][c4 + 3]};
-        *(float4*)&uT[((long)(b * D_INNER + db * 64 + dl) << 9) + lb * 64 + c4] = v;
+                Ct[tx * 4 + j][ty * 4 + i] = softplus_f(acc[i][j] + DTB[bn + tx * 4 + j]);
+        __syncthreads();
+        const int b = bm >> 9;
+        const int l0 = bm & 511;
+        const int r2 = tid >> 4;
+        const int c4 = (tid & 15) * 4;
+#pragma unroll
+        for (int q = 0; q < 4; ++q) {
+            const int dl = r2 + q * 16;
+            float4 v = {Ct[dl][c4], Ct[dl][c4 + 1], Ct[dl][c4 + 2], Ct[dl][c4 + 3]};
+            *(float4*)&dtT[((long)(b * D_INNER + bn + dl) << 9) + l0 + c4] = v;
+        }
+        __syncthreads();
     }
 }
 
@@ -650,159 +440,338 @@
     }
 }
 
-__global__ __launch_bounds__(256) void gate_kernel(
-    const float* __restrict__ ysT, const float* __restrict__ uT,
-    const float* __restrict__ Dp, const bf16* __restrict__ xz,
-    bf16* __restrict__ y)
-{
-    __shared__ float t[64][65];
-    __shared__ float t2[64][65];
-    const int db = blockIdx.x;
-    const int lb = blockIdx.y;
-    const int b  = blockIdx.z;
-    const int tid = threadIdx.x;
-    const int r  = tid >> 4;
-    const int c4 = (tid & 15) * 4;
-
-#pragma unroll
-    for (int q = 0; q < 4; ++q) {
-        const int dr = r + q * 16;
-        const long base = (((long)(b * D_INNER + db * 64 + dr)) << 9) + lb * 64 + c4;
-        const float4 v = *(const float4*)&ysT[base];
-        const float4 w = *(const float4*)&uT[base];
-        t[dr][c4 + 0] = v.x; t[dr][c4 + 1] = v.y;
-        t[dr][c4 + 2] = v.z; t[dr][c4 + 3] = v.w;
-        t2[dr][c4 + 0] = w.x; t2[dr][c4 + 1] = w.y;
-        t2[dr][c4 + 2] = w.z; t2[dr][c4 + 3] = w.w;
-    }
-    __syncthreads();
-
-    const float4 dp4 = *(const float4*)&Dp[db * 64 + c4];
-#pragma unroll
-    for (int q = 0; q < 4; ++q) {
-        const int lr = r + q * 16;
-        const long row = (long)b * L_SEQ + lb * 64 + lr;
-        const ushort4 zu = *(const ushort4*)&xz[row * 2 * D_INNER + D_INNER + db * 64 + c4];
-        const float r0 = (t[c4 + 0][lr] + t2[c4 + 0][lr] * dp4.x) * silu_f(bf2f(zu.x));
-        const float r1 = (t[c4 + 1][lr] + t2[c4 + 1][lr] * dp4.y) * silu_f(bf2f(zu.y));
-        const float r2 = (t[c4 + 2][lr] + t2[c4 + 2][lr] * dp4.z) * silu_f(bf2f(zu.z));
-        const float r3 = (t[c4 + 3][lr] + t2[c4 + 3][lr] * dp4.w) * silu_f(bf2f(zu.w));
-        bf16 b0 = __float2bfloat16(r0), b1 = __float2bfloat16(r1);
-        bf16 b2 = __float2bfloat16(r2), b3 = __float2bfloat16(r3);
-        ushort4 pk;
-        pk.x = *reinterpret_cast<unsigned short*>(&b0);
-        pk.y = *reinterpret_cast<unsigned short*>(&b1);
-        pk.z = *reinterpret_cast<unsigned short*>(&b2);
-        pk.w = *reinterpret_cast<unsigned short*>(&b3);
-        *reinterpret_cast<ushort4*>(y + row * D_INNER + db * 64 + c4) = pk;
-    }
-}
-
 #define QT 16
 #define CK 64
 
-__global__ __launch_bounds__(256) void attn_kernel(
-    const float* __restrict__ q, const float* __restrict__ k,
-    const float* __restrict__ v, bf16* __restrict__ o)
+__global__ __launch_bounds__(256, 4) void tail_fused(
+    const float* ysT, const float* uT, const float* DP, const bf16* xzb,
+    bf16* yb ,
+    const bf16* OPWb, const float* X, float* h1,
+    const float* n2a, const float* n2b, bf16* ln23,
+    const bf16* WQb, const float* WQB, float* qb,
+    const float* kb, const float* vbuf, bf16* aob,
+    const bf16* WOb, const float* WOB, float* h2,
+    const float* n3a, const float* n3b,
+    const bf16* W1b, const float* W1B,
+    const bf16* W2b, const float* W2B, float* outp)
 {
-    const int qt = blockIdx.x;
-    const int hh = blockIdx.y;
-    const int b  = blockIdx.z;
-    const int t = threadIdx.x;
-    const int lane = t & 15;
-    const int qa = t >> 4;
-    const int q0 = qt * QT + qa;
-
-    __shared__ float Ks[CK][36];
-    __shared__ float Vs[CK][36];
-
-    const float scale = 0.17677669529663687f;
-    float qr0[32];
-    {
-        const float* q0p = q + ((long)(b * L_SEQ + q0) * D_MODEL + hh * DK);
-#pragma unroll
-        for (int i = 0; i < 8; ++i) {
-            const float4 a = *(const float4*)&q0p[i * 4];
-            qr0[i*4+0] = a.x * scale; qr0[i*4+1] = a.y * scale;
-            qr0[i*4+2] = a.z * scale; qr0[i*4+3] = a.w * scale;
-        }
-    }
-
-    float m0 = -1e30f, l0 = 0.f, o0[32] = {};
-
-    for (int c = 0; c < L_SEQ; c += CK) {
-        __syncthreads();
+    cg::grid_group gg = cg::this_grid();
+    __shared__ float sm[8320];
+    const int tid = threadIdx.x;
+    const int NB = (int)gridDim.x;
+    const int lane = tid & 63;
+    const int wave = tid >> 6;
+    const int row16 = lane & 15;
+    const int quad  = lane >> 4;
+
+    for (int vb0 = (int)blockIdx.x; vb0 < 256; vb0 += NB) {
+        float (*tg)[65]  = (float(*)[65])sm;
+        float (*t2g)[65] = (float(*)[65])(sm + 4160);
+        const int db = vb0 & 15;
+        const int lb = (vb0 >> 4) & 7;
+        const int b  = vb0 >> 7;
+        const int r  = tid >> 4;
+        const int c4 = (tid & 15) * 4;
+#pragma unroll
+        for (int q = 0; q < 4; ++q) {
+            const int dr = r + q * 16;
+            const long base = (((long)(b * D_INNER + db * 64 + dr)) << 9) + lb * 64 + c4;
+            const float4 v = *(const float4*)&ysT[base];
+            const float4 w4 = *(const float4*)&uT[base];
+            tg[dr][c4 + 0] = v.x; tg[dr][c4 + 1] = v.y;
+            tg[dr][c4 + 2] = v.z; tg[dr][c4 + 3] = v.w;
+            t2g[dr][c4 + 0] = w4.x; t2g[dr][c4 + 1] = w4.y;
+            t2g[dr][c4 + 2] = w4.z; t2g[dr][c4 + 3] = w4.w;
+        }
+        __syncthreads();
+        const float4 dp4 = *(const float4*)&DP[db * 64 + c4];
+#pragma unroll
+        for (int q = 0; q < 4; ++q) {
+            const int lr = r + q * 16;
+            const long row = (long)b * L_SEQ + lb * 64 + lr;
+            const ushort4 zu = *(const ushort4*)&xzb[row * 2 * D_INNER + D_INNER + db * 64 + c4];
+            const float r0 = (tg[c4 + 0][lr] + t2g[c4 + 0][lr] * dp4.x) * silu_f(bf2f(zu.x));
+            const float r1 = (tg[c4 + 1][lr] + t2g[c4 + 1][lr] * dp4.y) * silu_f(bf2f(zu.y));
+            const float r2 = (tg[c4 + 2][lr] + t2g[c4 + 2][lr] * dp4.z) * silu_f(bf2f(zu.z));
+            const float r3 = (tg[c4 + 3][lr] + t2g[c4 + 3][lr] * dp4.w) * silu_f(bf2f(zu.w));
+            bf16 b0 = __float2bfloat16(r0), b1 = __float2bfloat16(r1);
+            bf16 b2 = __float2bfloat16(r2), b3 = __float2bfloat16(r3);
+            ushort4 pk;
+            pk.x = *reinterpret_cast<unsigned short*>(&b0);
+            pk.y = *reinterpret_cast<unsigned short*>(&b1);
+            pk.z = *reinterpret_cast<unsigned short*>(&b2);
+            pk.w = *reinterpret_cast<unsigned short*>(&b3);
+            *reinterpret_cast<ushort4*>(yb + row * D_INNER + db * 64 + c4) = pk;
+        }
+        __syncthreads();
+    }
+    gg.sync();
+
+    for (int vb0 = (int)blockIdx.x; vb0 < 256; vb0 += NB) {
+        const int bn = (vb0 & 3) * 64;
+        const int bm = ((vb0 >> 2) & 15) * 64 + wave * 16;
+        const int kz = vb0 >> 6;
+        floatx4 acc[4];
+#pragma unroll
+        for (int t = 0; t < 4; ++t) acc[t] = (floatx4){0.f, 0.f, 0.f, 0.f};
+        gemm64_body(yb, OPWb, D_INNER, kz * 256, kz * 256 + 256, bm, bn, D_MODEL, acc, lane);
+#pragma unroll
+        for (int t = 0; t < 4; ++t) {
+            const int gn = bn + t * 16 + row16;
+#pragma unroll
+            for (int r = 0; r < 4; ++r) {
+                const int gm = bm + quad * 4 + r;
+                float v = acc[t][r];
+                const long ci = (long)gm * D_MODEL + gn;
+                if (kz == 0) v += X[ci];
+                atomicAdd(&h1[ci], v);
+            }
+        }
+    }
+    gg.sync();
+
+    for (int vb0 = (int)blockIdx.x; vb0 < R_TOT; vb0 += NB) {
+        float* r1 = sm; float* r2 = sm + 256;
+        const float v = h1[(long)vb0 * D_MODEL + tid];
+        r1[tid] = v; r2[tid] = v * v;
+        __syncthreads();
+        for (int s = 128; s > 0; s >>= 1) {
+            if (tid < s) { r1[tid] += r1[tid + s]; r2[tid] += r2[tid + s]; }
+            __syncthreads();
+        }
+        const float mean = r1[0] * (1.f / 256.f);
+        const float var = (r2[0] - 256.f * mean * mean) * (1.f / 255.f);
+        const float sd = sqrtf(fmaxf(var, 0.f));
+        const float o = n2a[tid] * (v - mean) / (sd + 1e-6f) + n2b[tid];
+        ln23[(long)vb0 * D_MODEL + tid] = __float2bfloat16(o);
+        __syncthreads();
+    }
+    gg.sync();
+
+    for (int vb0 = (int)blockIdx.x; vb0 < 128; vb0 += NB) {
+        const int bn = (vb0 & 3) * 64;
+        const int bm = ((vb0 >> 2) & 15) * 64 + wave * 16;
+        const int kz = vb0 >> 6;
+        floatx4 acc[4];
+#pragma unroll
+        for (int t = 0; t < 4; ++t) acc[t] = (floatx4){0.f, 0.f, 0.f, 0.f};
+        gemm64_body(ln23, WQb, D_MODEL, kz * 128, kz * 128 + 128, bm, bn, D_MODEL, acc, lane);
+#pragma unroll
+        for (int t = 0; t < 4; ++t) {
+            const int gn = bn + t * 16 + row16;
+            const float bs = (kz == 0) ? WQB[gn] : 0.f;
+#pragma unroll
+            for (int r = 0; r < 4; ++r) {
+                const int gm = bm + quad * 4 + r;
+                atomicAdd(&qb[(long)gm * D_MODEL + gn], acc[t][r] + bs);
+            }
+        }
+    }
+    gg.sync();
+
+    for (int vb0 = (int)blockIdx.x; vb0 < 512; vb0 += NB) {
+        float (*Ks)[36] = (float(*)[36])sm;
+        float (*Vs)[36] = (float(*)[36])(sm + 2304);
+        const int qt = vb0 & 31;
+        const int hh = (vb0 >> 5) & 7;
+        const int b  = vb0 >> 8;
+        const int lane16 = tid & 15;
+        const int qa = tid >> 4;
+        const int q0 = qt * QT + qa;
+
+        const float scale = 0.17677669529663687f;
+        float qr0[32];
         {
-            const int fid = t * 2;
-            const int row = fid >> 3;
-            const int c0  = (fid & 7) * 4;
-            const float* kp = k + ((long)(b * L_SEQ + c + row) * D_MODEL + hh * DK + c0);
-            const float* vp = v + ((long)(b * L_SEQ + c + row) * D_MODEL + hh * DK + c0);
-            *(float4*)&Ks[row][c0]     = *(const float4*)kp;
-            *(float4*)&Ks[row][c0 + 4] = *(const float4*)(kp + 4);
-            *(float4*)&Vs[row][c0]     = *(const float4*)vp;
-            *(float4*)&Vs[row][c0 + 4] = *(const float4*)(vp + 4);
-        }
-        __syncthreads();
-
-        float s0[4];
-#pragma unroll
-        for (int i = 0; i < 4; ++i) {
-            const int kk = i * 16 + lane;
-            float a0 = 0.f;
-#pragma unroll
-            for (int dd = 0; dd < 32; dd += 4) {
-                const float4 kv = *(const float4*)&Ks[kk][dd];
-                a0 = fmaf(qr0[dd+0], kv.x, a0); a0 = fmaf(qr0[dd+1], kv.y, a0);
-                a0 = fmaf(qr0[dd+2], kv.z, a0); a0 = fmaf(qr0[dd+3], kv.w, a0);
-            }
-            s0[i] = a0;
-        }
-
-        float cm0 = s0[0];
-#pragma unroll
-        for (int i = 1; i < 4; ++i) cm0 = fmaxf(cm0, s0[i]);
-#pragma unroll
-        for (int off = 8; off > 0; off >>= 1)
-            cm0 = fmaxf(cm0, __shfl_down(cm0, off, 16));
-        cm0 = __shfl(cm0, 0, 16);
-
-        const float nm0 = fmaxf(m0, cm0);
-        const float al0 = fexp(m0 - nm0);
-        l0 *= al0;
-#pragma unroll
-        for (int dd = 0; dd < 32; ++dd) o0[dd] *= al0;
-        m0 = nm0;
-
-        float p0[4];
-#pragma unroll
-        for (int i = 0; i < 4; ++i) { p0[i] = fexp(s0[i] - m0); l0 += p0[i]; }
-
-#pragma unroll
-        for (int i = 0; i < 4; ++i) {
-            const int kk = i * 16 + lane;
-#pragma unroll
-            for (int dd = 0; dd < 32; dd += 4) {
-                const float4 vv = *(const float4*)&Vs[kk][dd];
-                o0[dd+0] = fmaf(p0[i], vv.x, o0[dd+0]);
-                o0[dd+1] = fmaf(p0[i], vv.y, o0[dd+1]);
-                o0[dd+2] = fmaf(p0[i], vv.z, o0[dd+2]);
-                o0[dd+3] = fmaf(p0[i], vv.w, o0[dd+3]);
-            }
-        }
-    }
-
-#pragma unroll
-    for (int off = 8; off > 0; off >>= 1) {
-        l0 += __shfl_down(l0, off, 16);
-#pragma unroll
-        for (int dd = 0; dd < 32; ++dd) o0[dd] += __shfl_down(o0[dd], off, 16);
-    }
-    if (lane == 0) {
-        const float i0 = 1.f / l0;
-        bf16* op0 = o + ((long)(b * L_SEQ + q0) * D_MODEL + hh * DK);
-#pragma unroll
-        for (int dd = 0; dd < 32; ++dd) op0[dd] = __float2bfloat16(o0[dd] * i0);
+            const float* q0p = qb + ((long)(b * L_SEQ + q0) * D_MODEL + hh * DK);
+#pragma unroll
+            for (int i = 0; i < 8; ++i) {
+                const float4 a = *(const float4*)&q0p[i * 4];
+                qr0[i*4+0] = a.x * scale; qr0[i*4+1] = a.y * scale;
+                qr0[i*4+2] = a.z * scale; qr0[i*4+3] = a.w * scale;
+            }
+        }
+        float m0 = -1e30f, l0 = 0.f, o0[32] = {};
+
+        for (int c = 0; c < L_SEQ; c += CK) {
+            __syncthreads();
+            {
+                const int fid = tid * 2;
+                const int row = fid >> 3;
+                const int c0  = (fid & 7) * 4;
+                const float* kp = kb + ((long)(b * L_SEQ + c + row) * D_MODEL + hh * DK + c0);
+                const float* vp = vbuf + ((long)(b * L_SEQ + c + row) * D_MODEL + hh * DK + c0);
+                *(float4*)&Ks[row][c0]     = *(const float4*)kp;
+                *(float4*)&Ks[row][c0 + 4] = *(const float4*)(kp + 4);
+                *(float4*)&Vs[row][c0]     = *(const float4*)vp;
+                *(float4*)&Vs[row][c0 + 4] = *(const float4*)(vp + 4);
+            }
+            __syncthreads();
+
+            float s0[4];
+#pragma unroll
+            for (int i = 0; i < 4; ++i) {
+                const int kk = i * 16 + lane16;
+                float a0 = 0.f;
+#pragma unroll
+                for (int dd = 0; dd < 32; dd += 4) {
+                    const float4 kv = *(const float4*)&Ks[kk][dd];
+                    a0 = fmaf(qr0[dd+0], kv.x, a0); a0 = fmaf(qr0[dd+1], kv.y, a0);
+                    a0 = fmaf(qr0[dd+2], kv.z, a0); a0 = fmaf(qr0[dd+3], kv.w, a0);
+                }
+                s0[i] = a0;
+            }
+            float cm0 = s0[0];
+#pragma unroll
+            for (int i = 1; i < 4; ++i) cm0 = fmaxf(cm0, s0[i]);
+#pragma unroll
+            for (int off = 8; off > 0; off >>= 1)
+                cm0 = fmaxf(cm0, __shfl_down(cm0, off, 16));
+            cm0 = __shfl(cm0, 0, 16);
+
+            const float nm0 = fmaxf(m0, cm0);
+            const float al0 = fexp(m0 - nm0);
+            l0 *= al0;
+#pragma unroll
+            for (int dd = 0; dd < 32; ++dd) o0[dd] *= al0;
+            m0 = nm0;
+
+            float p0[4];
+#pragma unroll
+            for (int i = 0; i < 4; ++i) { p0[i] = fexp(s0[i] - m0); l0 += p0[i]; }
+
+#pragma unroll
+            for (int i = 0; i < 4; ++i) {
+                const int kk = i * 16 + lane16;
+#pragma unroll
+                for (int dd = 0; dd < 32; dd += 4) {
+                    const float4 vv = *(const float4*)&Vs[kk][dd];
+                    o0[dd+0] = fmaf(p0[i], vv.x, o0[dd+0]);
+                    o0[dd+1] = fmaf(p0[i], vv.y, o0[dd+1]);
+                    o0[dd+2] = fmaf(p0[i], vv.z, o0[dd+2]);
+                    o0[dd+3] = fmaf(p0[i], vv.w, o0[dd+3]);
+                }
+            }
+        }
+#pragma unroll
+        for (int off = 8; off > 0; off >>= 1) {
+            l0 += __shfl_down(l0, off, 16);
+#pragma unroll
+            for (int dd = 0; dd < 32; ++dd) o0[dd] += __shfl_down(o0[dd], off, 16);
+        }
+        if (lane16 == 0) {
+            const float i0 = 1.f / l0;
+            bf16* op0 = aob + ((long)(b * L_SEQ + q0) * D_MODEL + hh * DK);
+#pragma unroll
+            for (int dd = 0; dd < 32; ++dd) op0[dd] = __float2bfloat16(o0[dd] * i0);
+        }
+        __syncthreads();
+    }
+    gg.sync();
+
+    for (int vb0 = (int)blockIdx.x; vb0 < R_TOT / 16; vb0 += NB) {
+        float (*tile)[264] = (float(*)[264])sm;
+        float* red1 = sm + 4224;
+        float* red2 = sm + 4480;
+        const int bm = vb0 * 16;
+
+        floatx4 acc[4];
+#pragma unroll
+        for (int t = 0; t < 4; ++t) acc[t] = (floatx4){0.f, 0.f, 0.f, 0.f};
+        const long arow = (long)(bm + row16) * D_MODEL;
+        for (int k0 = 0; k0 < D_MODEL; k0 += 32) {
+            const short8 av = *(const short8*)(aob + arow + k0 + quad * 8);
+#pragma unroll
+            for (int t = 0; t < 4; ++t) {
+                const int gn = wave * 64 + t * 16 + row16;
+                const short8 bv = *(const short8*)(WOb + (long)gn * D_MODEL + k0 + quad * 8);
+                acc[t] = __builtin_amdgcn_mfma_f32_16x16x32_bf16(av, bv, acc[t], 0, 0, 0);
+            }
+        }
+#pragma unroll
+        for (int t = 0; t < 4; ++t) {
+            const int gn = wave * 64 + t * 16 + row16;
+            const float bs = WOB[gn];
+#pragma unroll
+            for (int r = 0; r < 4; ++r) {
+                const int gm = bm + quad * 4 + r;
+                float v = acc[t][r] + bs;
+                const long ci = (long)gm * D_MODEL + gn;
+                v += h1[ci];
+                h2[ci] = v;
+                tile[quad * 4 + r][gn] = v;
+            }
+        }
+        __syncthreads();
+
+        const int r = tid >> 4;
+        const int g = tid & 15;
+        float sv = 0.f, qv = 0.f;
+#pragma unroll
+        for (int i = 0; i < 16; ++i) {
+            const float x = tile[r][g * 16 + i];
+            sv += x; qv += x * x;
+        }
+        red1[r * 16 + g] = sv; red2[r * 16 + g] = qv;
+        __syncthreads();
+        float ts = 0.f, tq = 0.f;
+#pragma unroll
+        for (int i = 0; i < 16; ++i) { ts += red1[r * 16 + i]; tq += red2[r * 16 + i]; }
+        const float mean = ts * (1.f / 256.f);
+        const float var = (tq - 256.f * mean * mean) * (1.f / 255.f);
+        const float sd = sqrtf(fmaxf(var, 0.f));
+        const long rowbase = (long)(bm + r) * D_MODEL;
+#pragma unroll
+        for (int i = 0; i < 16; ++i) {
+            const int c = g * 16 + i;
+            const float o = n3a[c] * (tile[r][c] - mean) / (sd + 1e-6f) + n3b[c];
+            ln23[rowbase + c] = __float2bfloat16(o);
+        }
+        __syncthreads();
+    }
+    gg.sync();
+
+    for (int vb0 = (int)blockIdx.x; vb0 < 256; vb0 += NB) {
+        const int bn = (vb0 & 15) * 64;
+        const int bm = (vb0 >> 4) * 64 + wave * 16;
+        floatx4 acc[4];
+#pragma unroll
+        for (int t = 0; t < 4; ++t) acc[t] = (floatx4){0.f, 0.f, 0.f, 0.f};
+        gemm64_body(ln23, W1b, D_MODEL, 0, D_MODEL, bm, bn, D_FF, acc, lane);
+#pragma unroll
+        for (int t = 0; t < 4; ++t) {
+            const int gn = bn + t * 16 + row16;
+            const float bs = W1B[gn];
+#pragma unroll
+            for (int r = 0; r < 4; ++r) {
+                const int gm = bm + quad * 4 + r;
+                const float v = fmaxf(acc[t][r] + bs, 0.f);
+                yb[(long)gm * D_FF + gn] = __float2bfloat16(v);
+            }
+        }
+    }
+    gg.sync();
+
+    for (int vb0 = (int)blockIdx.x; vb0 < 256; vb0 += NB) {
+        const int bn = (vb0 & 3) * 64;
+        const int bm = ((vb0 >> 2) & 15) * 64 + wave * 16;
+        const int kz = vb0 >> 6;
+        floatx4 acc[4];
+#pragma unroll
+        for (int t = 0; t < 4; ++t) acc[t] = (floatx4){0.f, 0.f, 0.f, 0.f};
+        gemm64_body(yb, W2b, D_FF, kz * 256, kz * 256 + 256, bm, bn, D_MODEL, acc, lane);
+#pragma unroll
+        for (int t = 0; t < 4; ++t) {
+            const int gn = bn + t * 16 + row16;
+            const float bs = (kz == 0) ? W2B[gn] : 0.f;
+#pragma unroll
+            for (int r = 0; r < 4; ++r) {
+                const int gm = bm + quad * 4 + r;
+                float v = acc[t][r] + bs;
+                const long ci = (long)gm * D_MODEL + gn;
+                if (kz == 0) v += h2[ci];
+                atomicAdd(&outp[ci], v);
+            }
+        }
     }
 }
 
@@ -844,12 +813,10 @@
     bf16* bp = (bf16*)d_ws;
     bf16* ub   = bp;  bp += (long)R_TOT * D_INNER;
     bf16* ybb  = bp;  bp += (long)R_TOT * D_INNER;
-    bf16* ffab = ybb;
     bf16* xzb  = bp;  bp += (long)R_TOT * 2 * D_INNER;
     bf16* ln1b = bp;  bp += (long)R_TOT * D_MODEL;
     bf16* aob  = ln1b;
     bf16* ln2b = bp;  bp += (long)R_TOT * D_MODEL;
-    bf16* ln3b = ln2b;
     bf16* arena = bp; bp += S_TOT;
     bf16* MEMb = arena;
     bf16* INWb = MEMb + S_MEM;
@@ -873,47 +840,44 @@
     float* vb  = p;                                  p += (long)R_TOT * D_MODEL;
     float* h2  = p;                                  p += (long)R_TOT * D_MODEL;
 
-    const dim3 blk256(256);
-    const int MT64 = R_TOT / 64;
-
-    pack_ln1<<<PACK_BLKS + R_TOT + ZERO_BLKS, blk256, 0, stream>>>(
-        MEM, INW, XPW, OPW, WQ, WKw, WVw, WO, W1, W2, arena,
-        X, N1A, N1B, ln1b, h1, out, dbl);
-
-    mfma_gemm<0><<<dim3(2 * D_INNER / 64, MT64), blk256, 0, stream>>>(
-        ln1b, INWb, D_MODEL, nullptr, xzb, 2 * D_INNER, nullptr, nullptr,
-        R_TOT, 2 * D_INNER);
-
-    conv_silu_T<<<dim3(D_INNER / 64, L_SEQ / 64, B_SZ), blk256, 0, stream>>>(
-        xzb, CW, CB, ub, uT);
-
-    xproj_kv_gemm<<<dim3((DBL_LD + 63) / 64, MT64, 8), blk256, 0, stream>>>(
-        ub, XPWb, dbl, MEMb, WKb, WVb, WKB, WVB, kb, vb);
-
-    dt_gemm_T<<<dim3(D_INNER / 64, MT64), blk256, 0, stream>>>(dbl, DTW, DTB, dtT);
+    int occH = 4, occT = 4;
+    (void)hipOccupancyMaxActiveBlocksPerMultiprocessor(&occH, head_fused, 256, 0);
+    (void)hipOccupancyMaxActiveBlocksPerMultiprocessor(&occT, tail_fused, 256, 0);
+    if (occH < 1) occH = 1;
+    if (occT < 1) occT = 1;
+    int gH = occH * 256; if (gH > 1024) gH = 1024;
+    int gT = occT * 256; if (gT > 1024) gT = 1024;
+
+    void* hargs[] = {
+        (void*)&MEM, (void*)&INW, (void*)&XPW, (void*)&OPW, (void*)&WQ,
+        (void*)&WKw, (void*)&WVw, (void*)&WO, (void*)&W1, (void*)&W2,
+        (void*)&arena,
+        (void*)&X, (void*)&N1A, (void*)&N1B, (void*)&ln1b,
+        (void*)&h1, (void*)&out, (void*)&dbl,
+        (void*)&INWb, (void*)&xzb,
+        (void*)&CW, (void*)&CB, (void*)&ub, (void*)&uT,
+        (void*)&XPWb, (void*)&dbl,
+        (void*)&MEMb, (void*)&WKb, (void*)&WVb,
+        (void*)&WKB, (void*)&WVB, (void*)&kb, (void*)&vb,
+        (void*)&DTW, (void*)&DTB, (void*)&dtT
+    };
+    (void)hipLaunchCooperativeKernel(head_fused, dim3(gH), dim3(256), hargs, 0, stream);
 
     scan_fused<<<B_SZ * D_INNER / DPB, dim3(1024), 0, stream>>>(dtT, uT, dbl, ALG, ysT);
 
-    gate_kernel<<<dim3(D_INNER / 64, L_SEQ / 64, B_SZ), blk256, 0, stream>>>(
-        ysT, uT, DP, xzb, ybb);
-
-    splitk_gemm<4><<<dim3(D_MODEL / 64, MT64, 4), blk256, 0, stream>>>(
-        ybb, OPWb, D_INNER, h1, D_MODEL, nullptr, X, R_TOT, D_MODEL);
-
-    ln_kernel<<<R_TOT, blk256, 0, stream>>>(h1, N2A, N2B, ln2b);
-
-    q_gemm<<<dim3(D_MODEL / 64, MT64, 2), blk256, 0, stream>>>(ln2b, WQb, WQB, qb);
-
-    attn_kernel<<<dim3(L_SEQ / QT, N_HEADS, B_SZ), blk256, 0, stream>>>(qb, kb, vb, aob);
-
-    gemm16_ln<<<R_TOT / 16, blk256, 0, stream>>>(
-        aob, WOb, D_MODEL, WOB, h1, h2, N3A, N3B, ln3b);
-
-    mfma_gemm<1><<<dim3(D_FF / 64, MT64), blk256, 0, stream>>>(
-        ln3b, W1b, D_MODEL, nullptr, ffab, D_FF, W1B, nullptr, R_TOT, D_FF);
-
-    splitk_gemm<4><<<dim3(D_MODEL / 64, MT64, 4), blk256, 0, stream>>>(
-        ffab, W2b, D_FF, out, D_MODEL, W2B, h2, R_TOT, D_MODEL);
+    void* targs[] = {
+        (void*)&ysT, (void*)&uT, (void*)&DP, (void*)&xzb,
+        (void*)&ybb,
+        (void*)&OPWb, (void*)&X, (void*)&h1,
+        (void*)&N2A, (void*)&N2B, (void*)&ln2b,
+        (void*)&WQb, (void*)&WQB, (void*)&qb,
+        (void*)&kb, (void*)&vb, (void*)&aob,
+        (void*)&WOb, (void*)&WOB, (void*)&h2,
+        (void*)&N3A, (void*)&N3B,
+        (void*)&W1b, (void*)&W1B,
+        (void*)&W2b, (void*)&W2B, (void*)&out
+    };
+    (void)hipLaunchCooperativeKernel(tail_fused, dim3(gT), dim3(256), targs, 0, stream);
 
     (void)in_sizes; (void)n_in; (void)out_size; (void)ws_size;
 }
```

New measurement: 995.2 us. 3.09x slower.
